# Kernel optimization log

Hardware: AMD Instinct MI355X
Metric: run time of the kernel (lower is better)

## Reference

```python
import jax, jax.numpy as jnp
import numpy as np

N_ENT = 40000
N_REL2 = 500      # num_rel * 2
E_DIR = 200000
E_2HOP = 50000
D_IN = 128        # entity/relation init dim
D_EMB = 256       # embed_dim
N_HEADS = 4
N_HID = D_EMB // N_HEADS  # 64
LRELU_ALPHA = 0.2
BN_EPS = 1e-5


def setup_inputs() -> dict:
    key = jax.random.key(0)
    ks = jax.random.split(key, 13)
    s = 0.1  # weight init scale
    return {
        "edge_index": jax.random.randint(ks[0], (2, E_DIR), 0, N_ENT),
        "edge_type": jax.random.randint(ks[1], (E_DIR,), 0, N_REL2),
        "indices_2hop": jax.random.randint(ks[2], (E_2HOP, 4), 0, N_REL2),
        "init_embed": jax.random.normal(ks[3], (N_ENT, D_IN), jnp.float32) * s,
        "init_rel": jax.random.normal(ks[4], (N_REL2, D_IN), jnp.float32) * s,
        "W_heads": jax.random.normal(ks[5], (N_HEADS, 2 * D_IN + D_IN, N_HID), jnp.float32) * s,
        "a_heads": jax.random.normal(ks[6], (N_HEADS, N_HID, 1), jnp.float32) * s,
        "gat_W": jax.random.normal(ks[7], (D_IN, D_EMB), jnp.float32) * s,
        "out_W": jax.random.normal(ks[8], (2 * D_EMB + D_EMB, D_EMB), jnp.float32) * s,
        "out_a": jax.random.normal(ks[9], (D_EMB, 1), jnp.float32) * s,
        "W_entities": jax.random.normal(ks[10], (D_IN, D_EMB), jnp.float32) * s,
        "bn_gamma": jnp.ones((D_EMB,), jnp.float32),
        "bn_beta": jnp.zeros((D_EMB,), jnp.float32),
    }


def segment_softmax(logits, idx, num_seg):
    # sparse softmax grouped by idx (PyG-style): subtract per-segment max, exp, normalize
    m = jax.ops.segment_max(logits, idx, num_segments=num_seg)
    e = jnp.exp(logits - m[idx])
    s = jax.ops.segment_sum(e, idx, num_segments=num_seg)
    return e / (s[idx] + 1e-16)


def reference(edge_index, edge_type, indices_2hop, init_embed, init_rel,
              W_heads, a_heads, gat_W, out_W, out_a, W_entities, bn_gamma, bn_beta):
    n = init_embed.shape[0]
    # build full edge list: flipped direct edges + 2-hop edges
    edge_nhop = jnp.stack([indices_2hop[:, 3], indices_2hop[:, 0]])  # [2, E2]
    ei = jnp.concatenate([edge_index[::-1], edge_nhop], axis=1)      # [2, Etot]
    row, col = ei[0], ei[1]
    t0, t1 = indices_2hop[:, 1], indices_2hop[:, 2]

    # first-layer edge relation embeddings
    edge_embed = jnp.concatenate([init_rel[edge_type], init_rel[t0] + init_rel[t1]], axis=0)
    feat = jnp.concatenate([init_embed[row], init_embed[col], edge_embed], axis=1)  # [Etot, 3*D_IN]

    def head(W, a):
        eh = feat @ W                                     # [Etot, N_HID]
        logit = jax.nn.leaky_relu((eh @ a)[:, 0], LRELU_ALPHA)
        alpha = segment_softmax(logit, row, n)
        agg = jax.ops.segment_sum(alpha[:, None] * eh, row, num_segments=n)
        return jax.nn.elu(agg)                            # concat=True -> elu

    x = jax.vmap(head)(W_heads, a_heads)                  # [H, N, N_HID]
    x = jnp.transpose(x, (1, 0, 2)).reshape(n, -1)        # [N, H*N_HID]

    r = init_rel @ gat_W                                  # [R2, D_EMB]
    edge_embed2 = jnp.concatenate([r[edge_type], r[t0] + r[t1]], axis=0)
    feat2 = jnp.concatenate([x[row], x[col], edge_embed2], axis=1)  # [Etot, 3*D_EMB]
    eh2 = feat2 @ out_W                                   # [Etot, D_EMB]
    logit2 = jax.nn.leaky_relu((eh2 @ out_a)[:, 0], LRELU_ALPHA)
    alpha2 = segment_softmax(logit2, row, n)
    out = jax.ops.segment_sum(alpha2[:, None] * eh2, row, num_segments=n)
    x = jax.nn.elu(out)                                   # elu applied in GAT.forward

    x = x + init_embed @ W_entities
    # BatchNorm1d (training-mode batch stats, biased variance)
    mu = jnp.mean(x, axis=0)
    var = jnp.var(x, axis=0)
    x = (x - mu) / jnp.sqrt(var + BN_EPS) * bn_gamma + bn_beta
    return x, r
```

## Files before the change

kernel.cpp:

```cpp
#include <hip/hip_runtime.h>
#include <hip/hip_bf16.h>
#include <math.h>

#define N_ENT 40000
#define N_REL 500
#define E_DIR 200000
#define E_2HOP 50000
#define E_TOT 250000
#define D_IN 128
#define D_EMB 256
#define LRELU 0.2f
#define BN_EPS 1e-5f
#define NB_SCAN 157
#define NB_DIR 782
#define NB2 8
#define E2PB 6250
#define N_HEAVY 500
#define DEG_SPLIT 32

typedef __hip_bfloat16 bf16;
typedef __attribute__((ext_vector_type(8))) short short8;
typedef __attribute__((ext_vector_type(4))) float float4v;

__device__ __forceinline__ float b2f(bf16 v){ return __bfloat162float(v); }
__device__ __forceinline__ float bitsf(unsigned int u){ return __builtin_bit_cast(float, u); }
__device__ __forceinline__ unsigned short bbits(float v){ return __builtin_bit_cast(unsigned short, __float2bfloat16(v)); }

__global__ void prep_hist(const float* __restrict__ Wh, const float* __restrict__ ow,
                          const float* __restrict__ we, const float* __restrict__ emb,
                          bf16* __restrict__ WAp, bf16* __restrict__ WBp, bf16* __restrict__ WEp,
                          bf16* __restrict__ OWp0, bf16* __restrict__ OWp1, float* __restrict__ WC,
                          bf16* __restrict__ embb,
                          const int* __restrict__ ei, const int* __restrict__ i2,
                          int* __restrict__ cnt, int* __restrict__ H2){
  __shared__ int hc[512];
  const int HS = 384*64;
  int b = blockIdx.x, tid = threadIdx.x;
  if (b < NB_DIR){
    int e = b*256 + tid;
    if (e < E_DIR) atomicAdd(&cnt[ei[E_DIR + e]], 1);
    return;
  }
  b -= NB_DIR;
  if (b < NB2){
    hc[tid] = 0; hc[tid + 256] = 0;
    __syncthreads();
    int base = b*E2PB;
    for (int it = 0; it < 25; it++){
      int o2 = it*256 + tid;
      if (o2 < E2PB){
        int r = i2[(base + o2)*4 + 3];
        atomicAdd(&hc[r], 1);
      }
    }
    __syncthreads();
    for (int r = tid; r < 500; r += 256) H2[b*500 + r] = hc[r];
    return;
  }
  b -= NB2;
  if (b >= 240){
    int i = (b - 240)*256 + tid;
    embb[i] = __float2bfloat16(emb[i]);
    return;
  }
  if (b < 112){
    int seg, base;
    if      (b < 16){ seg = 0; base = 0; }
    else if (b < 32){ seg = 1; base = 16; }
    else if (b < 48){ seg = 2; base = 32; }
    else if (b < 80){ seg = 3; base = 48; }
    else            { seg = 4; base = 80; }
    int idx = (b - base)*256 + tid;
    int lane = idx & 63, nt = (idx >> 6) & 15, kc = idx >> 10;
    int quad = lane >> 4, l16 = lane & 15;
    int col = nt*16 + l16;
    int kbase = kc*32 + quad*8;
    bf16* dst = (seg==0?WAp : seg==1?WBp : seg==2?WEp : seg==3?OWp0 : OWp1) + (size_t)idx*8;
    #pragma unroll
    for (int j = 0; j < 8; j++){
      int k = kbase + j;
      float v;
      if      (seg == 0) v = Wh[(col>>6)*HS + k*64 + (col&63)];
      else if (seg == 1) v = Wh[(col>>6)*HS + (k+128)*64 + (col&63)];
      else if (seg == 2) v = we[(size_t)k*256 + col];
      else if (seg == 3) v = ow[(size_t)k*256 + col];
      else               v = ow[(size_t)(k+256)*256 + col];
      dst[j] = __float2bfloat16(v);
    }
  } else {
    int idx = (b - 112)*256 + tid;
    int k = idx >> 8, col = idx & 255;
    WC[idx] = Wh[(col>>6)*HS + (k+256)*64 + (col&63)];
  }
}

__global__ void h2scan(const int* __restrict__ H2, int* __restrict__ b2off, int* __restrict__ c2){
  int r = threadIdx.x;
  if (r < 500){
    int s = 0;
    #pragma unroll
    for (int b = 0; b < NB2; b++){ b2off[b*500 + r] = s; s += H2[b*500 + r]; }
    c2[r] = s;
  }
}

__global__ void scan_bsum(const int* __restrict__ cnt, const int* __restrict__ c2,
                          int* __restrict__ bsum){
  int i = blockIdx.x*256 + threadIdx.x;
  int v = 0;
  if (i < N_ENT){ v = cnt[i]; if (i < 500) v += c2[i]; }
  int lane = threadIdx.x & 63, w = threadIdx.x >> 6;
  int s = v;
  #pragma unroll
  for (int o = 32; o >= 1; o >>= 1) s += __shfl_xor(s, o, 64);
  __shared__ int ws[4];
  if (lane == 0) ws[w] = s;
  __syncthreads();
  if (threadIdx.x == 0) bsum[blockIdx.x] = ws[0]+ws[1]+ws[2]+ws[3];
}

__global__ __launch_bounds__(256) void scan_final2(const int* __restrict__ cnt,
    const int* __restrict__ c2, const int* __restrict__ bsum, int* __restrict__ off){
  __shared__ int boffs[NB_SCAN];
  __shared__ int ws4[4];
  __shared__ int ws2[4];
  __shared__ int totals;
  int t = threadIdx.x;
  int lane = t & 63, w = t >> 6;
  {
    int v = (t < NB_SCAN) ? bsum[t] : 0;
    int s = v;
    #pragma unroll
    for (int o = 1; o < 64; o <<= 1){ int n = __shfl_up(s, o, 64); if (lane >= o) s += n; }
    if (lane == 63) ws4[w] = s;
    __syncthreads();
    int add = 0;
    for (int k = 0; k < w; k++) add += ws4[k];
    int incl = s + add;
    if (t < NB_SCAN) boffs[t] = incl - v;
    if (t == NB_SCAN-1) totals = incl;
  }
  __syncthreads();
  int i = blockIdx.x*256 + t;
  int v = 0;
  if (i < N_ENT){ v = cnt[i]; if (i < 500) v += c2[i]; }
  int s = v;
  #pragma unroll
  for (int o = 1; o < 64; o <<= 1){ int n = __shfl_up(s, o, 64); if (lane >= o) s += n; }
  if (lane == 63) ws2[w] = s;
  __syncthreads();
  int add = boffs[blockIdx.x];
  for (int k = 0; k < w; k++) add += ws2[k];
  if (i < N_ENT) off[i] = add + s - v;
  if (blockIdx.x == 0 && t == 0) off[N_ENT] = totals;
}

__device__ __forceinline__ void mfma_panel(const short* __restrict__ A,
    const short* __restrict__ Bp, bf16* __restrict__ C, int K,
    const float* __restrict__ avec, float* __restrict__ Sout, int dmode,
    int bx, int half){
  int w = threadIdx.x >> 6, lane = threadIdx.x & 63;
  int quad = lane >> 4, l16 = lane & 15;
  int rm = bx*64 + w*16;
  int arow = rm + l16;
  float4v acc[8];
  #pragma unroll
  for (int nt = 0; nt < 8; nt++) acc[nt] = (float4v){0.f,0.f,0.f,0.f};
  int nkc = K >> 5;
  const short8* Ap = (const short8*)(A + (size_t)arow*K);
  const short8* Bv = (const short8*)Bp + half*512 + lane;
  short8 a_cur = Ap[quad];
  for (int kc = 0; kc < nkc; kc++){
    int kn = (kc + 1 < nkc) ? kc + 1 : kc;
    short8 a_nxt = Ap[kn*4 + quad];
    const short8* bp = Bv + (size_t)kc*1024;
    short8 b[4];
    #pragma unroll
    for (int nt = 0; nt < 4; nt++) b[nt] = bp[nt*64];
    #pragma unroll
    for (int nt = 0; nt < 4; nt++)
      acc[nt] = __builtin_amdgcn_mfma_f32_16x16x32_bf16(a_cur, b[nt], acc[nt], 0, 0, 0);
    #pragma unroll
    for (int nt = 0; nt < 4; nt++) b[nt] = bp[(nt+4)*64];
    #pragma unroll
    for (int nt = 0; nt < 4; nt++)
      acc[nt+4] = __builtin_amdgcn_mfma_f32_16x16x32_bf16(a_cur, b[nt], acc[nt+4], 0, 0, 0);
    a_cur = a_nxt;
  }
  #pragma unroll
  for (int nt = 0; nt < 8; nt++){
    int col = (half*8 + nt)*16 + l16;
    #pragma unroll
    for (int r = 0; r < 4; r++)
      C[(size_t)(rm + quad*4 + r)*256 + col] = __float2bfloat16(acc[nt][r]);
  }
  if (Sout){
    if (dmode == 0){
      #pragma unroll
      for (int hl = 0; hl < 2; hl++){
        float pr[4] = {0.f,0.f,0.f,0.f};
        #pragma unroll
        for (int ntl = 0; ntl < 4; ntl++){
          int ln = hl*4 + ntl;
          float av = avec[(half*8 + ln)*16 + l16];
          #pragma unroll
          for (int r = 0; r < 4; r++) pr[r] += acc[ln][r]*av;
        }
        #pragma unroll
        for (int m = 8; m >= 1; m >>= 1)
          #pragma unroll
          for (int r = 0; r < 4; r++) pr[r] += __shfl_xor(pr[r], m, 64);
        if (l16 == 0){
          #pragma unroll
          for (int r = 0; r < 4; r++)
            Sout[(rm + quad*4 + r)*4 + half*2 + hl] = pr[r];
        }
      }
    } else {
      float pr[4] = {0.f,0.f,0.f,0.f};
      #pragma unroll
      for (int ln = 0; ln < 8; ln++){
        float av = avec[(half*8 + ln)*16 + l16];
        #pragma unroll
        for (int r = 0; r < 4; r++) pr[r] += acc[ln][r]*av;
      }
      #pragma unroll
      for (int m = 8; m >= 1; m >>= 1)
        #pragma unroll
        for (int r = 0; r < 4; r++) pr[r] += __shfl_xor(pr[r], m, 64);
      if (l16 == 0){
        #pragma unroll
        for (int r = 0; r < 4; r++) atomicAdd(&Sout[rm + quad*4 + r], pr[r]);
      }
    }
  }
}

__device__ __forceinline__ void gemm64_body(const float* __restrict__ A,
    const float* __restrict__ B, float* __restrict__ C, bf16* __restrict__ Cb,
    int M, int K, const float* __restrict__ av, float* __restrict__ So, int mode,
    int bxx, int byy, char* smem){
  const int N = 256;
  float (*As)[65] = (float (*)[65])smem;
  float (*Bsf)[65] = (float (*)[65])(smem + 16*65*sizeof(float));
  int bm = bxx * 64, bn = byy * 64;
  int tid = threadIdx.x;
  int tx = tid & 15, ty = tid >> 4;
  float acc[4][4] = {};
  for (int k0 = 0; k0 < K; k0 += 16){
    #pragma unroll
    for (int j = 0; j < 4; j++){
      int idx = tid + j*256;
      int m = idx >> 4, kk = idx & 15;
      int gm = bm + m;
      float v = 0.f;
      if (gm < M) v = A[(size_t)gm*K + k0 + kk];
      As[kk][m] = v;
    }
    #pragma unroll
    for (int j = 0; j < 4; j++){
      int idx = tid + j*256;
      int kk = idx >> 6, n = idx & 63;
      Bsf[kk][n] = B[(size_t)(k0+kk)*N + bn + n];
    }
    __syncthreads();
    #pragma unroll
    for (int kk = 0; kk < 16; kk++){
      float a[4], b[4];
      #pragma unroll
      for (int i = 0; i < 4; i++) a[i] = As[kk][ty*4+i];
      #pragma unroll
      for (int j = 0; j < 4; j++) b[j] = Bsf[kk][tx*4+j];
      #pragma unroll
      for (int i = 0; i < 4; i++)
        #pragma unroll
        for (int j = 0; j < 4; j++) acc[i][j] += a[i]*b[j];
    }
    __syncthreads();
  }
  if (Cb){
    #pragma unroll
    for (int i = 0; i < 4; i++){
      int gm = bm + ty*4 + i;
      if (gm >= M) continue;
      #pragma unroll
      for (int j = 0; j < 4; j++)
        Cb[(size_t)gm*N + bn + tx*4 + j] = __float2bfloat16(acc[i][j]);
    }
  } else {
    #pragma unroll
    for (int i = 0; i < 4; i++){
      int gm = bm + ty*4 + i;
      if (gm >= M) continue;
      #pragma unroll
      for (int j = 0; j < 4; j++)
        C[(size_t)gm*N + bn + tx*4 + j] = acc[i][j];
    }
  }
  if (mode != 2){
    float pr[4];
    #pragma unroll
    for (int i = 0; i < 4; i++){
      float p = 0.f;
      #pragma unroll
      for (int j = 0; j < 4; j++) p += acc[i][j]*av[bn + tx*4 + j];
      pr[i] = p;
    }
    #pragma unroll
    for (int m = 8; m >= 1; m >>= 1)
      #pragma unroll
      for (int i = 0; i < 4; i++) pr[i] += __shfl_xor(pr[i], m, 64);
    if (tx == 0){
      #pragma unroll
      for (int i = 0; i < 4; i++){
        int gm = bm + ty*4 + i;
        if (gm < M){
          if (mode == 0) So[gm*4 + byy] = pr[i];
          else atomicAdd(&So[gm], pr[i]);
        }
      }
    }
  }
}

__global__ __launch_bounds__(256, 4) void mega1(
    const short* __restrict__ embb, const short* __restrict__ WAp, const short* __restrict__ WBp,
    const short* __restrict__ WEp, bf16* __restrict__ P1, bf16* __restrict__ P2, bf16* __restrict__ EP,
    const float* __restrict__ ah, float* __restrict__ S1, float* __restrict__ S2,
    const float* __restrict__ rel, const float* __restrict__ WC, const float* __restrict__ gw,
    float* __restrict__ RF, float* __restrict__ SRm, bf16* __restrict__ PRb,
    const int* __restrict__ ei, const int* __restrict__ et, const int* __restrict__ i2,
    const int* __restrict__ off, int* __restrict__ cur, const int* __restrict__ b2off,
    int4* __restrict__ EIDX, int useEP){
  __shared__ char smem[8704];
  __shared__ int lc[512];
  int x = blockIdx.x, tid = threadIdx.x;
  if (x < NB_DIR){
    int e = x*256 + tid;
    if (e < E_DIR){
      int r = ei[E_DIR + e];
      int p = atomicAdd(&cur[r], 1);
      int4 v; v.x = ei[e]; v.y = et[e]; v.z = -1; v.w = r;
      EIDX[off[r] + p] = v;
    }
    return;
  }
  x -= NB_DIR;
  if (x < NB2){
    lc[tid] = 0; lc[tid + 256] = 0;
    __syncthreads();
    int base = x*E2PB;
    for (int it = 0; it < 25; it++){
      int o2 = it*256 + tid;
      if (o2 < E2PB){
        int e2 = base + o2;
        int q = e2*4;
        int r = i2[q + 3];
        int myp = atomicAdd(&lc[r], 1);
        int d = off[r+1] - 1 - (b2off[x*500 + r] + myp);
        int4 v; v.x = i2[q]; v.y = i2[q+1]; v.z = i2[q+2]; v.w = r;
        EIDX[d] = v;
      }
    }
    return;
  }
  x -= NB2;
  if (x < 64){
    int z = x >> 5, rr = x & 31, by = rr >> 3, bx = rr & 7;
    if (z == 0) gemm64_body(rel, WC, nullptr, PRb, N_REL, 128, ah, SRm, 0, bx, by, smem);
    else        gemm64_body(rel, gw, RF, nullptr, N_REL, 128, nullptr, nullptr, 2, bx, by, smem);
    return;
  }
  x -= 64;
  int p = x / 1250, rest = x % 1250;
  if (p == 2 && !useEP) return;
  const short* B = p==0 ? WAp : (p==1 ? WBp : WEp);
  bf16* C = p==0 ? P1 : (p==1 ? P2 : EP);
  float* S = p==0 ? S1 : (p==1 ? S2 : nullptr);
  mfma_panel(embb, B, C, 128, ah, S, 0, rest >> 1, rest & 1);
}

__global__ __launch_bounds__(256, 4) void mega2(
    const short* __restrict__ X1s, const short* __restrict__ OWp0, const short* __restrict__ OWp1,
    bf16* __restrict__ Q1, bf16* __restrict__ Q2, const float* __restrict__ oa,
    float* __restrict__ S1B, float* __restrict__ S2B,
    const float* __restrict__ RF, const float* __restrict__ owB, float* __restrict__ SRB,
    bf16* __restrict__ QRb){
  __shared__ char smem[8704];
  int x = blockIdx.x;
  if (x < 32){
    int by = x >> 3, bx = x & 7;
    gemm64_body(RF, owB, nullptr, QRb, N_REL, 256, oa, SRB, 1, bx, by, smem);
    return;
  }
  x -= 32;
  int p = x / 1250, rest = x % 1250;
  mfma_panel(X1s, p==0 ? OWp0 : OWp1, p==0 ? Q1 : Q2, 256, oa,
             p==0 ? S1B : S2B, 1, rest >> 1, rest & 1);
}

__global__ void gemm64_acc(const float* __restrict__ A, const float* __restrict__ B,
                           float* __restrict__ C, int M, int K){
  const int N = 256;
  __shared__ float As[16][65];
  __shared__ float Bs[16][65];
  int bm = blockIdx.x * 64, bn = blockIdx.y * 64;
  int tid = threadIdx.x;
  int tx = tid & 15, ty = tid >> 4;
  float acc[4][4] = {};
  for (int k0 = 0; k0 < K; k0 += 16){
    #pragma unroll
    for (int j = 0; j < 4; j++){
      int idx = tid + j*256;
      int m = idx >> 4, kk = idx & 15;
      int gm = bm + m;
      float v = 0.f;
      if (gm < M) v = A[(size_t)gm*K + k0 + kk];
      As[kk][m] = v;
    }
    #pragma unroll
    for (int j = 0; j < 4; j++){
      int idx = tid + j*256;
      int kk = idx >> 6, n = idx & 63;
      Bs[kk][n] = B[(size_t)(k0+kk)*N + bn + n];
    }
    __syncthreads();
    #pragma unroll
    for (int kk = 0; kk < 16; kk++){
      float a[4], b[4];
      #pragma unroll
      for (int i = 0; i < 4; i++) a[i] = As[kk][ty*4+i];
      #pragma unroll
      for (int j = 0; j < 4; j++) b[j] = Bs[kk][tx*4+j];
      #pragma unroll
      for (int i = 0; i < 4; i++)
        #pragma unroll
        for (int j = 0; j < 4; j++) acc[i][j] += a[i]*b[j];
    }
    __syncthreads();
  }
  #pragma unroll
  for (int i = 0; i < 4; i++){
    int gm = bm + ty*4 + i;
    if (gm >= M) continue;
    #pragma unroll
    for (int j = 0; j < 4; j++){
      size_t o = (size_t)gm*N + bn + tx*4 + j;
      C[o] += acc[i][j];
    }
  }
}

__global__ __launch_bounds__(256) void sm1f(const int* __restrict__ off, const int4* __restrict__ EIDX,
    const float* __restrict__ s1, const float* __restrict__ s2, const float* __restrict__ sR,
    float* __restrict__ L1, float* __restrict__ AS1, float* __restrict__ IV1){
  if (blockIdx.x < N_HEAVY){
    int i = blockIdx.x;
    int st = off[i], en = off[i+1];
    if (en - st <= DEG_SPLIT) return;
    int h = threadIdx.x >> 6, lane = threadIdx.x & 63;
    float* Lh = L1 + (size_t)h*E_TOT;
    float si = s1[i*4 + h];
    float mx = -1e30f;
    for (int t = st + lane; t < en; t += 64){
      int4 e = EIDX[t];
      float v = si + s2[e.x*4+h] + sR[e.y*4+h];
      if (e.z >= 0) v += sR[e.z*4+h];
      v = (v >= 0.f) ? v : LRELU*v;
      Lh[t] = v;
      mx = fmaxf(mx, v);
    }
    #pragma unroll
    for (int o = 32; o >= 1; o >>= 1) mx = fmaxf(mx, __shfl_xor(mx, o, 64));
    float sm = 0.f;
    for (int t = st + lane; t < en; t += 64){
      float ev = __expf(Lh[t] - mx); Lh[t] = ev; sm += ev;
    }
    #pragma unroll
    for (int o = 32; o >= 1; o >>= 1) sm += __shfl_xor(sm, o, 64);
    float inv = 1.f/(sm + 1e-16f);
    if (lane == 0){ AS1[i*4+h] = sm*inv; IV1[i*4+h] = inv; }
    return;
  }
  int wid = threadIdx.x >> 6, lane = threadIdx.x & 63;
  int i = (blockIdx.x - N_HEAVY)*4 + wid;
  if (i >= N_ENT) return;
  int st = off[i], en = off[i+1];
  if (i < N_HEAVY && en - st > DEG_SPLIT) return;
  int hf = lane >> 4, l16 = lane & 15;
  float* Lh = L1 + (size_t)hf*E_TOT;
  float si = s1[i*4 + hf];
  if (en - st > 2*16){
    float mx = -1e30f;
    for (int t = st + l16; t < en; t += 16){
      int4 e = EIDX[t];
      float v = si + s2[e.x*4+hf] + sR[e.y*4+hf];
      if (e.z >= 0) v += sR[e.z*4+hf];
      v = (v >= 0.f) ? v : LRELU*v;
      Lh[t] = v; mx = fmaxf(mx, v);
    }
    #pragma unroll
    for (int o = 8; o >= 1; o >>= 1) mx = fmaxf(mx, __shfl_xor(mx, o, 64));
    float sm = 0.f;
    for (int t = st + l16; t < en; t += 16){
      float ev = __expf(Lh[t] - mx); Lh[t] = ev; sm += ev;
    }
    #pragma unroll
    for (int o = 8; o >= 1; o >>= 1) sm += __shfl_xor(sm, o, 64);
    float inv = 1.f/(sm + 1e-16f);
    if (l16 == 0){ AS1[i*4+hf] = sm*inv; IV1[i*4+hf] = inv; }
    return;
  }
  int t0 = st + l16, t1 = t0 + 16;
  float v0 = -1e30f, v1 = -1e30f;
  if (t0 < en){
    int4 e = EIDX[t0];
    float v = si + s2[e.x*4+hf] + sR[e.y*4+hf];
    if (e.z >= 0) v += sR[e.z*4+hf];
    v0 = (v >= 0.f) ? v : LRELU*v;
  }
  if (t1 < en){
    int4 e = EIDX[t1];
    float v = si + s2[e.x*4+hf] + sR[e.y*4+hf];
    if (e.z >= 0) v += sR[e.z*4+hf];
    v1 = (v >= 0.f) ? v : LRELU*v;
  }
  float mx = fmaxf(v0, v1);
  #pragma unroll
  for (int o = 8; o >= 1; o >>= 1) mx = fmaxf(mx, __shfl_xor(mx, o, 64));
  float sm = 0.f;
  if (t0 < en){ float ev = __expf(v0 - mx); Lh[t0] = ev; sm += ev; }
  if (t1 < en){ float ev = __expf(v1 - mx); Lh[t1] = ev; sm += ev; }
  #pragma unroll
  for (int o = 8; o >= 1; o >>= 1) sm += __shfl_xor(sm, o, 64);
  float inv = 1.f/(sm + 1e-16f);
  if (l16 == 0){ AS1[i*4+hf] = sm*inv; IV1[i*4+hf] = inv; }
}

__global__ __launch_bounds__(256) void sm2f(const int* __restrict__ off, const int4* __restrict__ EIDX,
    const float* __restrict__ s1, const float* __restrict__ s2, const float* __restrict__ sR,
    float* __restrict__ L2, float* __restrict__ AS2, float* __restrict__ IV2){
  __shared__ float wsm[4], wss[4];
  if (blockIdx.x < N_HEAVY){
    int i = blockIdx.x;
    int st = off[i], en = off[i+1];
    if (en - st <= DEG_SPLIT) return;
    int tid = threadIdx.x, w = tid >> 6, lane = tid & 63;
    float si = s1[i];
    float mx = -1e30f;
    for (int t = st + tid; t < en; t += 256){
      int4 e = EIDX[t];
      float v = si + s2[e.x] + sR[e.y];
      if (e.z >= 0) v += sR[e.z];
      v = (v >= 0.f) ? v : LRELU*v;
      L2[t] = v; mx = fmaxf(mx, v);
    }
    #pragma unroll
    for (int o = 32; o >= 1; o >>= 1) mx = fmaxf(mx, __shfl_xor(mx, o, 64));
    if (lane == 0) wsm[w] = mx;
    __syncthreads();
    mx = fmaxf(fmaxf(wsm[0], wsm[1]), fmaxf(wsm[2], wsm[3]));
    float sm = 0.f;
    for (int t = st + tid; t < en; t += 256){
      float ev = __expf(L2[t] - mx); L2[t] = ev; sm += ev;
    }
    #pragma unroll
    for (int o = 32; o >= 1; o >>= 1) sm += __shfl_xor(sm, o, 64);
    if (lane == 0) wss[w] = sm;
    __syncthreads();
    sm = wss[0]+wss[1]+wss[2]+wss[3];
    float inv = 1.f/(sm + 1e-16f);
    if (tid == 0){ AS2[i] = sm*inv; IV2[i] = inv; }
    return;
  }
  int wid = threadIdx.x >> 6, lane = threadIdx.x & 63;
  int i = (blockIdx.x - N_HEAVY)*4 + wid;
  if (i >= N_ENT) return;
  int st = off[i], en = off[i+1];
  if (i < N_HEAVY && en - st > DEG_SPLIT) return;
  float si = s1[i];
  if (en - st > 64){
    float mx = -1e30f;
    for (int t = st + lane; t < en; t += 64){
      int4 e = EIDX[t];
      float v = si + s2[e.x] + sR[e.y];
      if (e.z >= 0) v += sR[e.z];
      v = (v >= 0.f) ? v : LRELU*v;
      L2[t] = v; mx = fmaxf(mx, v);
    }
    #pragma unroll
    for (int o = 32; o >= 1; o >>= 1) mx = fmaxf(mx, __shfl_xor(mx, o, 64));
    float sm = 0.f;
    for (int t = st + lane; t < en; t += 64){
      float ev = __expf(L2[t] - mx); L2[t] = ev; sm += ev;
    }
    #pragma unroll
    for (int o = 32; o >= 1; o >>= 1) sm += __shfl_xor(sm, o, 64);
    float inv = 1.f/(sm + 1e-16f);
    if (lane == 0){ AS2[i] = sm*inv; IV2[i] = inv; }
    return;
  }
  int t0 = st + lane;
  float v0 = -1e30f;
  if (t0 < en){
    int4 e = EIDX[t0];
    float v = si + s2[e.x] + sR[e.y];
    if (e.z >= 0) v += sR[e.z];
    v0 = (v >= 0.f) ? v : LRELU*v;
  }
  float mx = v0;
  #pragma unroll
  for (int o = 32; o >= 1; o >>= 1) mx = fmaxf(mx, __shfl_xor(mx, o, 64));
  float sm = 0.f;
  if (t0 < en){ float ev = __expf(v0 - mx); L2[t0] = ev; sm += ev; }
  #pragma unroll
  for (int o = 32; o >= 1; o >>= 1) sm += __shfl_xor(sm, o, 64);
  float inv = 1.f/(sm + 1e-16f);
  if (lane == 0){ AS2[i] = sm*inv; IV2[i] = inv; }
}

#define UNPK(u, r0, r1, r2, r3) \
  r0 = bitsf((u).x << 16); r1 = bitsf((u).x & 0xffff0000u); \
  r2 = bitsf((u).y << 16); r3 = bitsf((u).y & 0xffff0000u);

__global__ __launch_bounds__(256) void agg1(const int* __restrict__ off,
    const int4* __restrict__ EIDX, const float* __restrict__ W1, const float* __restrict__ AS1,
    const float* __restrict__ IV1,
    const bf16* __restrict__ P1, const bf16* __restrict__ P2, const bf16* __restrict__ PRm,
    bf16* __restrict__ X1){
  __shared__ float red[4][256];
  if (blockIdx.x < N_HEAVY){
    int i = blockIdx.x;
    int st = off[i], en = off[i+1];
    if (en - st <= DEG_SPLIT) return;
    int w = threadIdx.x >> 6, lane = threadIdx.x & 63;
    int hf = lane >> 4, f0 = lane*4;
    size_t ob = (size_t)i*256 + f0;
    const float* Wp = W1 + (size_t)hf*E_TOT;
    float a0=0,a1=0,a2=0,a3=0;
    for (int t = st + w*4; t < en; t += 16){
      int4 e[4]; float wv[4]; uint2 u[4]; uint2 rr[4];
      #pragma unroll
      for (int k = 0; k < 4; k++){
        int tt = t + k;
        bool vld = tt < en;
        int tc = vld ? tt : st;
        e[k] = EIDX[tc]; wv[k] = vld ? Wp[tc] : 0.f;
      }
      #pragma unroll
      for (int k = 0; k < 4; k++){
        u[k] = *(const uint2*)(P2 + (size_t)e[k].x*256 + f0);
        rr[k] = *(const uint2*)(PRm + (size_t)e[k].y*256 + f0);
      }
      float rf[4][4];
      #pragma unroll
      for (int k = 0; k < 4; k++){ UNPK(rr[k], rf[k][0], rf[k][1], rf[k][2], rf[k][3]) }
      #pragma unroll
      for (int k = 0; k < 4; k++){
        if (e[k].z >= 0){
          uint2 s = *(const uint2*)(PRm + (size_t)e[k].z*256 + f0);
          float s0,s1,s2,s3; UNPK(s, s0,s1,s2,s3)
          rf[k][0] += s0; rf[k][1] += s1; rf[k][2] += s2; rf[k][3] += s3;
        }
      }
      #pragma unroll
      for (int k = 0; k < 4; k++){
        a0 += wv[k]*(bitsf(u[k].x << 16) + rf[k][0]);
        a1 += wv[k]*(bitsf(u[k].x & 0xffff0000u) + rf[k][1]);
        a2 += wv[k]*(bitsf(u[k].y << 16) + rf[k][2]);
        a3 += wv[k]*(bitsf(u[k].y & 0xffff0000u) + rf[k][3]);
      }
    }
    *(float4*)&red[w][f0] = (float4){a0, a1, a2, a3};
    __syncthreads();
    if (w == 0){
      float4 r1 = *(float4*)&red[1][f0];
      float4 r2 = *(float4*)&red[2][f0];
      float4 r3 = *(float4*)&red[3][f0];
      a0 += r1.x + r2.x + r3.x;
      a1 += r1.y + r2.y + r3.y;
      a2 += r1.z + r2.z + r3.z;
      a3 += r1.w + r2.w + r3.w;
      float iv = IV1[i*4 + hf];
      a0 *= iv; a1 *= iv; a2 *= iv; a3 *= iv;
      float as = AS1[i*4 + hf];
      uint2 up = *(const uint2*)(P1 + ob);
      a0 += as*bitsf(up.x << 16);
      a1 += as*bitsf(up.x & 0xffff0000u);
      a2 += as*bitsf(up.y << 16);
      a3 += as*bitsf(up.y & 0xffff0000u);
      a0 = (a0 > 0.f) ? a0 : __expf(a0)-1.f;
      a1 = (a1 > 0.f) ? a1 : __expf(a1)-1.f;
      a2 = (a2 > 0.f) ? a2 : __expf(a2)-1.f;
      a3 = (a3 > 0.f) ? a3 : __expf(a3)-1.f;
      unsigned int lo = (unsigned int)bbits(a0) | ((unsigned int)bbits(a1) << 16);
      unsigned int hi = (unsigned int)bbits(a2) | ((unsigned int)bbits(a3) << 16);
      *(uint2*)(X1 + ob) = (uint2){lo, hi};
    }
    return;
  }
  int wid = threadIdx.x >> 6, lane = threadIdx.x & 63;
  int i = (blockIdx.x - N_HEAVY)*4 + wid;
  if (i >= N_ENT) return;
  int st = off[i], en = off[i+1];
  if (i < N_HEAVY && en - st > DEG_SPLIT) return;
  int hf = lane >> 4, f0 = lane*4;
  size_t ob = (size_t)i*256 + f0;
  if (st == en){
    *(uint2*)(X1 + ob) = (uint2){0u, 0u};
    return;
  }
  const float* Wp = W1 + (size_t)hf*E_TOT;
  float a0=0,a1=0,a2=0,a3=0;
  int t = st;
  int n4 = st + ((en - st) & ~3);
  for (; t < n4; t += 4){
    int4 e[4]; float wv[4]; uint2 u[4]; uint2 rr[4];
    #pragma unroll
    for (int k = 0; k < 4; k++){ e[k] = EIDX[t+k]; wv[k] = Wp[t+k]; }
    #pragma unroll
    for (int k = 0; k < 4; k++){
      u[k] = *(const uint2*)(P2 + (size_t)e[k].x*256 + f0);
      rr[k] = *(const uint2*)(PRm + (size_t)e[k].y*256 + f0);
    }
    float rf[4][4];
    #pragma unroll
    for (int k = 0; k < 4; k++){ UNPK(rr[k], rf[k][0], rf[k][1], rf[k][2], rf[k][3]) }
    #pragma unroll
    for (int k = 0; k < 4; k++){
      if (e[k].z >= 0){
        uint2 s = *(const uint2*)(PRm + (size_t)e[k].z*256 + f0);
        float s0,s1,s2,s3; UNPK(s, s0,s1,s2,s3)
        rf[k][0] += s0; rf[k][1] += s1; rf[k][2] += s2; rf[k][3] += s3;
      }
    }
    #pragma unroll
    for (int k = 0; k < 4; k++){
      a0 += wv[k]*(bitsf(u[k].x << 16) + rf[k][0]);
      a1 += wv[k]*(bitsf(u[k].x & 0xffff0000u) + rf[k][1]);
      a2 += wv[k]*(bitsf(u[k].y << 16) + rf[k][2]);
      a3 += wv[k]*(bitsf(u[k].y & 0xffff0000u) + rf[k][3]);
    }
  }
  for (; t < en; t++){
    float w = Wp[t];
    int4 e = EIDX[t];
    uint2 u = *(const uint2*)(P2 + (size_t)e.x*256 + f0);
    uint2 rr = *(const uint2*)(PRm + (size_t)e.y*256 + f0);
    float r0,r1,r2,r3; UNPK(rr, r0,r1,r2,r3)
    if (e.z >= 0){
      uint2 s = *(const uint2*)(PRm + (size_t)e.z*256 + f0);
      float s0,s1,s2,s3; UNPK(s, s0,s1,s2,s3)
      r0 += s0; r1 += s1; r2 += s2; r3 += s3;
    }
    a0 += w*(bitsf(u.x << 16) + r0);
    a1 += w*(bitsf(u.x & 0xffff0000u) + r1);
    a2 += w*(bitsf(u.y << 16) + r2);
    a3 += w*(bitsf(u.y & 0xffff0000u) + r3);
  }
  float iv = IV1[i*4 + hf];
  a0 *= iv; a1 *= iv; a2 *= iv; a3 *= iv;
  float as = AS1[i*4 + hf];
  uint2 up = *(const uint2*)(P1 + ob);
  a0 += as*bitsf(up.x << 16);
  a1 += as*bitsf(up.x & 0xffff0000u);
  a2 += as*bitsf(up.y << 16);
  a3 += as*bitsf(up.y & 0xffff0000u);
  a0 = (a0 > 0.f) ? a0 : __expf(a0)-1.f;
  a1 = (a1 > 0.f) ? a1 : __expf(a1)-1.f;
  a2 = (a2 > 0.f) ? a2 : __expf(a2)-1.f;
  a3 = (a3 > 0.f) ? a3 : __expf(a3)-1.f;
  unsigned int lo = (unsigned int)bbits(a0) | ((unsigned int)bbits(a1) << 16);
  unsigned int hi = (unsigned int)bbits(a2) | ((unsigned int)bbits(a3) << 16);
  *(uint2*)(X1 + ob) = (uint2){lo, hi};
}

__global__ __launch_bounds__(256) void agg2(const int* __restrict__ off,
    const int4* __restrict__ EIDX, const float* __restrict__ W2, const float* __restrict__ AS2,
    const float* __restrict__ IV2,
    const bf16* __restrict__ Q1, const bf16* __restrict__ Q2, const bf16* __restrict__ QRm,
    const bf16* __restrict__ EP, float* __restrict__ X2){
  __shared__ float red[4][256];
  if (blockIdx.x < N_HEAVY){
    int i = blockIdx.x;
    int st = off[i], en = off[i+1];
    if (en - st <= DEG_SPLIT) return;
    int w = threadIdx.x >> 6, lane = threadIdx.x & 63;
    int f0 = lane*4;
    size_t ob = (size_t)i*256 + f0;
    float a0=0,a1=0,a2=0,a3=0;
    for (int t = st + w*4; t < en; t += 16){
      int4 e[4]; float wv[4]; uint2 u[4]; uint2 rr[4];
      #pragma unroll
      for (int k = 0; k < 4; k++){
        int tt = t + k;
        bool vld = tt < en;
        int tc = vld ? tt : st;
        e[k] = EIDX[tc]; wv[k] = vld ? W2[tc] : 0.f;
      }
      #pragma unroll
      for (int k = 0; k < 4; k++){
        u[k] = *(const uint2*)(Q2 + (size_t)e[k].x*256 + f0);
        rr[k] = *(const uint2*)(QRm + (size_t)e[k].y*256 + f0);
      }
      float rf[4][4];
      #pragma unroll
      for (int k = 0; k < 4; k++){ UNPK(rr[k], rf[k][0], rf[k][1], rf[k][2], rf[k][3]) }
      #pragma unroll
      for (int k = 0; k < 4; k++){
        if (e[k].z >= 0){
          uint2 s = *(const uint2*)(QRm + (size_t)e[k].z*256 + f0);
          float s0,s1,s2,s3; UNPK(s, s0,s1,s2,s3)
          rf[k][0] += s0; rf[k][1] += s1; rf[k][2] += s2; rf[k][3] += s3;
        }
      }
      #pragma unroll
      for (int k = 0; k < 4; k++){
        a0 += wv[k]*(bitsf(u[k].x << 16) + rf[k][0]);
        a1 += wv[k]*(bitsf(u[k].x & 0xffff0000u) + rf[k][1]);
        a2 += wv[k]*(bitsf(u[k].y << 16) + rf[k][2]);
        a3 += wv[k]*(bitsf(u[k].y & 0xffff0000u) + rf[k][3]);
      }
    }
    *(float4*)&red[w][f0] = (float4){a0, a1, a2, a3};
    __syncthreads();
    if (w == 0){
      float4 r1 = *(float4*)&red[1][f0];
      float4 r2 = *(float4*)&red[2][f0];
      float4 r3 = *(float4*)&red[3][f0];
      a0 += r1.x + r2.x + r3.x;
      a1 += r1.y + r2.y + r3.y;
      a2 += r1.z + r2.z + r3.z;
      a3 += r1.w + r2.w + r3.w;
      float iv = IV2[i];
      a0 *= iv; a1 *= iv; a2 *= iv; a3 *= iv;
      float ep0=0.f, ep1=0.f, ep2=0.f, ep3=0.f;
      if (EP){
        uint2 ue = *(const uint2*)(EP + ob);
        ep0 = bitsf(ue.x << 16); ep1 = bitsf(ue.x & 0xffff0000u);
        ep2 = bitsf(ue.y << 16); ep3 = bitsf(ue.y & 0xffff0000u);
      }
      float as = AS2[i];
      uint2 uq = *(const uint2*)(Q1 + ob);
      a0 += as*bitsf(uq.x << 16);
      a1 += as*bitsf(uq.x & 0xffff0000u);
      a2 += as*bitsf(uq.y << 16);
      a3 += as*bitsf(uq.y & 0xffff0000u);
      a0 = ((a0 > 0.f) ? a0 : __expf(a0)-1.f) + ep0;
      a1 = ((a1 > 0.f) ? a1 : __expf(a1)-1.f) + ep1;
      a2 = ((a2 > 0.f) ? a2 : __expf(a2)-1.f) + ep2;
      a3 = ((a3 > 0.f) ? a3 : __expf(a3)-1.f) + ep3;
      *(float4*)(X2 + ob) = (float4){a0, a1, a2, a3};
    }
    return;
  }
  int wid = threadIdx.x >> 6, lane = threadIdx.x & 63;
  int i = (blockIdx.x - N_HEAVY)*4 + wid;
  if (i >= N_ENT) return;
  int st = off[i], en = off[i+1];
  if (i < N_HEAVY && en - st > DEG_SPLIT) return;
  int f0 = lane*4;
  size_t ob = (size_t)i*256 + f0;
  float ep0=0.f, ep1=0.f, ep2=0.f, ep3=0.f;
  if (EP){
    uint2 ue = *(const uint2*)(EP + ob);
    ep0 = bitsf(ue.x << 16); ep1 = bitsf(ue.x & 0xffff0000u);
    ep2 = bitsf(ue.y << 16); ep3 = bitsf(ue.y & 0xffff0000u);
  }
  if (st == en){
    *(float4*)(X2 + ob) = (float4){ep0, ep1, ep2, ep3};
    return;
  }
  float a0=0,a1=0,a2=0,a3=0;
  int t = st;
  int n4 = st + ((en - st) & ~3);
  for (; t < n4; t += 4){
    int4 e[4]; float wv[4]; uint2 u[4]; uint2 rr[4];
    #pragma unroll
    for (int k = 0; k < 4; k++){ e[k] = EIDX[t+k]; wv[k] = W2[t+k]; }
    #pragma unroll
    for (int k = 0; k < 4; k++){
      u[k] = *(const uint2*)(Q2 + (size_t)e[k].x*256 + f0);
      rr[k] = *(const uint2*)(QRm + (size_t)e[k].y*256 + f0);
    }
    float rf[4][4];
    #pragma unroll
    for (int k = 0; k < 4; k++){ UNPK(rr[k], rf[k][0], rf[k][1], rf[k][2], rf[k][3]) }
    #pragma unroll
    for (int k = 0; k < 4; k++){
      if (e[k].z >= 0){
        uint2 s = *(const uint2*)(QRm + (size_t)e[k].z*256 + f0);
        float s0,s1,s2,s3; UNPK(s, s0,s1,s2,s3)
        rf[k][0] += s0; rf[k][1] += s1; rf[k][2] += s2; rf[k][3] += s3;
      }
    }
    #pragma unroll
    for (int k = 0; k < 4; k++){
      a0 += wv[k]*(bitsf(u[k].x << 16) + rf[k][0]);
      a1 += wv[k]*(bitsf(u[k].x & 0xffff0000u) + rf[k][1]);
      a2 += wv[k]*(bitsf(u[k].y << 16) + rf[k][2]);
      a3 += wv[k]*(bitsf(u[k].y & 0xffff0000u) + rf[k][3]);
    }
  }
  for (; t < en; t++){
    float w = W2[t];
    int4 e = EIDX[t];
    uint2 u = *(const uint2*)(Q2 + (size_t)e.x*256 + f0);
    uint2 rr = *(const uint2*)(QRm + (size_t)e.y*256 + f0);
    float r0,r1,r2,r3; UNPK(rr, r0,r1,r2,r3)
    if (e.z >= 0){
      uint2 s = *(const uint2*)(QRm + (size_t)e.z*256 + f0);
      float s0,s1,s2,s3; UNPK(s, s0,s1,s2,s3)
      r0 += s0; r1 += s1; r2 += s2; r3 += s3;
    }
    a0 += w*(bitsf(u.x << 16) + r0);
    a1 += w*(bitsf(u.x & 0xffff0000u) + r1);
    a2 += w*(bitsf(u.y << 16) + r2);
    a3 += w*(bitsf(u.y & 0xffff0000u) + r3);
  }
  float iv = IV2[i];
  a0 *= iv; a1 *= iv; a2 *= iv; a3 *= iv;
  float as = AS2[i];
  uint2 uq = *(const uint2*)(Q1 + ob);
  a0 += as*bitsf(uq.x << 16);
  a1 += as*bitsf(uq.x & 0xffff0000u);
  a2 += as*bitsf(uq.y << 16);
  a3 += as*bitsf(uq.y & 0xffff0000u);
  a0 = ((a0 > 0.f) ? a0 : __expf(a0)-1.f) + ep0;
  a1 = ((a1 > 0.f) ? a1 : __expf(a1)-1.f) + ep1;
  a2 = ((a2 > 0.f) ? a2 : __expf(a2)-1.f) + ep2;
  a3 = ((a3 > 0.f) ? a3 : __expf(a3)-1.f) + ep3;
  *(float4*)(X2 + ob) = (float4){a0, a1, a2, a3};
}

__global__ void bn_reduce(const float* __restrict__ X, float* __restrict__ sums, float* __restrict__ sq){
  int ch = threadIdx.x;
  float s = 0.f, q = 0.f;
  for (int r = blockIdx.x; r < N_ENT; r += gridDim.x){
    float v = X[(size_t)r*256 + ch];
    s += v; q += v*v;
  }
  atomicAdd(&sums[ch], s);
  atomicAdd(&sq[ch], q);
}

__global__ void bn_final_r(float* __restrict__ X, const float* __restrict__ sums, const float* __restrict__ sq,
                           const float* __restrict__ gamma, const float* __restrict__ beta,
                           const float* __restrict__ RF, float* __restrict__ out_r){
  int b = blockIdx.x;
  if (b < 40000){
    int idx = b*256 + threadIdx.x;
    int ch = idx & 255;
    const float invn = 1.f/(float)N_ENT;
    float mean = sums[ch] * invn;
    float var  = fmaxf(sq[ch] * invn - mean*mean, 0.f);
    X[idx] = (X[idx] - mean) * rsqrtf(var + BN_EPS) * gamma[ch] + beta[ch];
  } else {
    int idx = (b - 40000)*256 + threadIdx.x;
    out_r[idx] = RF[idx];
  }
}

extern "C" void kernel_launch(void* const* d_in, const int* in_sizes, int n_in,
                              void* d_out, int out_size, void* d_ws, size_t ws_size,
                              hipStream_t stream){
  const int*   ei  = (const int*)d_in[0];
  const int*   et  = (const int*)d_in[1];
  const int*   i2  = (const int*)d_in[2];
  const float* emb = (const float*)d_in[3];
  const float* rel = (const float*)d_in[4];
  const float* Wh  = (const float*)d_in[5];
  const float* ah  = (const float*)d_in[6];
  const float* gw  = (const float*)d_in[7];
  const float* ow  = (const float*)d_in[8];
  const float* oa  = (const float*)d_in[9];
  const float* we  = (const float*)d_in[10];
  const float* gma = (const float*)d_in[11];
  const float* bta = (const float*)d_in[12];
  float* out = (float*)d_out;

  char* ws = (char*)d_ws;
  size_t o = 0;
  auto alloc = [&](size_t bytes)->char*{
    char* p = ws + o; o = (o + bytes + 255) & ~(size_t)255; return p;
  };
  bf16*  P1  = (bf16*)alloc(20480000);
  bf16*  P2  = (bf16*)alloc(20480000);
  bf16*  PRb = (bf16*)alloc(256000);
  bf16*  QRb = (bf16*)alloc(256000);
  float* RF  = (float*)alloc(512000);
  float* WC  = (float*)alloc(131072);
  bf16*  WAp = (bf16*)alloc(65536);
  bf16*  WBp = (bf16*)alloc(65536);
  bf16*  WEp = (bf16*)alloc(65536);
  bf16*  OWp0= (bf16*)alloc(131072);
  bf16*  OWp1= (bf16*)alloc(131072);
  float* S1  = (float*)alloc(640000);
  float* S2  = (float*)alloc(640000);
  float* SRm = (float*)alloc(8192);
  float* S1B = (float*)alloc(160000);
  float* S2B = (float*)alloc(160000);
  int*   CNT = (int*)alloc(160000);
  int*   CUR = (int*)alloc(160000);
  float* SRB = (float*)alloc(2048);
  float* BNS = (float*)alloc(1024);
  float* BNQ = (float*)alloc(1024);
  int*   OFF = (int*)alloc(160016);
  int*   BSUM= (int*)alloc(1024);
  int*   H2  = (int*)alloc(16000);
  int*   B2O = (int*)alloc(16000);
  int*   C2  = (int*)alloc(2048);
  int4*  EIDX= (int4*)alloc(4000000);
  float* L1  = (float*)alloc(4000000);
  float* L2  = (float*)alloc(1000000);
  float* AS1 = (float*)alloc(640000);
  float* AS2 = (float*)alloc(160000);
  float* IV1 = (float*)alloc(640000);
  float* IV2 = (float*)alloc(160000);
  size_t base_end = o;
  bool useEP = (ws_size >= base_end + 20480256 + 512);
  bf16* EP = nullptr;
  if (useEP) EP = (bf16*)alloc(20480000);
  bf16* X1b  = (bf16*)out;
  bf16* embb = (bf16*)((char*)out + 20480000);
  float* X2 = out;
  (void)in_sizes; (void)n_in; (void)out_size;

  hipMemsetAsync(S1B, 0, 644096, stream);

  prep_hist<<<NB_DIR + NB2 + 20240, 256, 0, stream>>>(Wh, ow, we, emb,
      WAp, WBp, WEp, OWp0, OWp1, WC, embb, ei, i2, CNT, H2);

  h2scan<<<1, 512, 0, stream>>>(H2, B2O, C2);
  scan_bsum<<<NB_SCAN, 256, 0, stream>>>(CNT, C2, BSUM);
  scan_final2<<<NB_SCAN, 256, 0, stream>>>(CNT, C2, BSUM, OFF);

  mega1<<<NB_DIR + NB2 + 64 + 3750, 256, 0, stream>>>(
      (const short*)embb, (const short*)WAp, (const short*)WBp, (const short*)WEp,
      P1, P2, EP, ah, S1, S2,
      rel, WC, gw, RF, SRm, PRb,
      ei, et, i2, OFF, CUR, B2O, EIDX, useEP ? 1 : 0);

  sm1f<<<N_HEAVY + N_ENT/4, 256, 0, stream>>>(OFF, EIDX, S1, S2, SRm, L1, AS1, IV1);
  agg1<<<N_HEAVY + N_ENT/4, 256, 0, stream>>>(OFF, EIDX, L1, AS1, IV1, P1, P2, PRb, X1b);

  mega2<<<32 + 2500, 256, 0, stream>>>(
      (const short*)X1b, (const short*)OWp0, (const short*)OWp1,
      P1, P2, oa, S1B, S2B, RF, ow + 131072, SRB, QRb);

  sm2f<<<N_HEAVY + N_ENT/4, 256, 0, stream>>>(OFF, EIDX, S1B, S2B, SRB, L2, AS2, IV2);
  agg2<<<N_HEAVY + N_ENT/4, 256, 0, stream>>>(OFF, EIDX, L2, AS2, IV2, P1, P2, QRb, EP, X2);

  if (!useEP)
    gemm64_acc<<<dim3((N_ENT+63)/64, 4), 256, 0, stream>>>(emb, we, X2, N_ENT, 128);

  bn_reduce<<<1024, 256, 0, stream>>>(X2, BNS, BNQ);
  bn_final_r<<<40500, 256, 0, stream>>>(X2, BNS, BNQ, gma, bta, RF, out + (size_t)N_ENT*256);
}
```

Before: 373.9 us.

## Fuse segment softmax into aggregation kernels for both GAT layers

Result: faster. 353.2 us (-5.5%).

```diff
diff --git a/kernel.cpp b/kernel.cpp
--- a/kernel.cpp
+++ b/kernel.cpp
@@ -17,6 +17,8 @@
 #define E2PB 6250
 #define N_HEAVY 500
 #define DEG_SPLIT 32
+#define HM1 512
+#define HM2 1024
 
 typedef __hip_bfloat16 bf16;
 typedef __attribute__((ext_vector_type(8))) short short8;
@@ -451,35 +453,131 @@
   }
 }
 
-__global__ __launch_bounds__(256) void sm1f(const int* __restrict__ off, const int4* __restrict__ EIDX,
+#define UNPK(u, r0, r1, r2, r3) \
+  r0 = bitsf((u).x << 16); r1 = bitsf((u).x & 0xffff0000u); \
+  r2 = bitsf((u).y << 16); r3 = bitsf((u).y & 0xffff0000u);
+
+__global__ __launch_bounds__(256) void fag1(const int* __restrict__ off,
+    const int4* __restrict__ EIDX,
     const float* __restrict__ s1, const float* __restrict__ s2, const float* __restrict__ sR,
-    float* __restrict__ L1, float* __restrict__ AS1, float* __restrict__ IV1){
+    const bf16* __restrict__ P1, const bf16* __restrict__ P2, const bf16* __restrict__ PRm,
+    bf16* __restrict__ X1){
+  __shared__ float red[4][256];
+  __shared__ float wE[4][HM1];
+  __shared__ float hsum[4], hmx[4];
   if (blockIdx.x < N_HEAVY){
     int i = blockIdx.x;
     int st = off[i], en = off[i+1];
     if (en - st <= DEG_SPLIT) return;
-    int h = threadIdx.x >> 6, lane = threadIdx.x & 63;
-    float* Lh = L1 + (size_t)h*E_TOT;
-    float si = s1[i*4 + h];
-    float mx = -1e30f;
-    for (int t = st + lane; t < en; t += 64){
-      int4 e = EIDX[t];
-      float v = si + s2[e.x*4+h] + sR[e.y*4+h];
-      if (e.z >= 0) v += sR[e.z*4+h];
-      v = (v >= 0.f) ? v : LRELU*v;
-      Lh[t] = v;
-      mx = fmaxf(mx, v);
-    }
-    #pragma unroll
-    for (int o = 32; o >= 1; o >>= 1) mx = fmaxf(mx, __shfl_xor(mx, o, 64));
-    float sm = 0.f;
-    for (int t = st + lane; t < en; t += 64){
-      float ev = __expf(Lh[t] - mx); Lh[t] = ev; sm += ev;
-    }
-    #pragma unroll
-    for (int o = 32; o >= 1; o >>= 1) sm += __shfl_xor(sm, o, 64);
-    float inv = 1.f/(sm + 1e-16f);
-    if (lane == 0){ AS1[i*4+h] = sm*inv; IV1[i*4+h] = inv; }
+    int w = threadIdx.x >> 6, lane = threadIdx.x & 63;
+    {
+      float si = s1[i*4 + w];
+      float mx = -1e30f;
+      for (int t = st + lane; t < en; t += 64){
+        int4 e = EIDX[t];
+        float v = si + s2[e.x*4+w] + sR[e.y*4+w];
+        if (e.z >= 0) v += sR[e.z*4+w];
+        v = (v >= 0.f) ? v : LRELU*v;
+        int idx = t - st;
+        if (idx < HM1) wE[w][idx] = v;
+        mx = fmaxf(mx, v);
+      }
+      #pragma unroll
+      for (int o = 32; o >= 1; o >>= 1) mx = fmaxf(mx, __shfl_xor(mx, o, 64));
+      float sm = 0.f;
+      for (int t = st + lane; t < en; t += 64){
+        int idx = t - st;
+        float v;
+        if (idx < HM1) v = wE[w][idx];
+        else {
+          int4 e = EIDX[t];
+          v = si + s2[e.x*4+w] + sR[e.y*4+w];
+          if (e.z >= 0) v += sR[e.z*4+w];
+          v = (v >= 0.f) ? v : LRELU*v;
+        }
+        float ev = __expf(v - mx);
+        if (idx < HM1) wE[w][idx] = ev;
+        sm += ev;
+      }
+      #pragma unroll
+      for (int o = 32; o >= 1; o >>= 1) sm += __shfl_xor(sm, o, 64);
+      if (lane == 0){ hsum[w] = sm; hmx[w] = mx; }
+    }
+    __syncthreads();
+    int hf = lane >> 4, f0 = lane*4;
+    size_t ob = (size_t)i*256 + f0;
+    float si2 = s1[i*4 + hf], mxh = hmx[hf];
+    float a0=0,a1=0,a2=0,a3=0;
+    for (int t = st + w*4; t < en; t += 16){
+      int4 e[4]; float wv[4]; uint2 u[4]; uint2 rr[4];
+      #pragma unroll
+      for (int k = 0; k < 4; k++){
+        int tt = t + k;
+        bool vld = tt < en;
+        int tc = vld ? tt : st;
+        e[k] = EIDX[tc];
+        int idx = tc - st;
+        float wt;
+        if (idx < HM1) wt = wE[hf][idx];
+        else {
+          float v = si2 + s2[e[k].x*4+hf] + sR[e[k].y*4+hf];
+          if (e[k].z >= 0) v += sR[e[k].z*4+hf];
+          v = (v >= 0.f) ? v : LRELU*v;
+          wt = __expf(v - mxh);
+        }
+        wv[k] = vld ? wt : 0.f;
+      }
+      #pragma unroll
+      for (int k = 0; k < 4; k++){
+        u[k] = *(const uint2*)(P2 + (size_t)e[k].x*256 + f0);
+        rr[k] = *(const uint2*)(PRm + (size_t)e[k].y*256 + f0);
+      }
+      float rf[4][4];
+      #pragma unroll
+      for (int k = 0; k < 4; k++){ UNPK(rr[k], rf[k][0], rf[k][1], rf[k][2], rf[k][3]) }
+      #pragma unroll
+      for (int k = 0; k < 4; k++){
+        if (e[k].z >= 0){
+          uint2 s = *(const uint2*)(PRm + (size_t)e[k].z*256 + f0);
+          float s0,ss1,ss2,s3; UNPK(s, s0,ss1,ss2,s3)
+          rf[k][0] += s0; rf[k][1] += ss1; rf[k][2] += ss2; rf[k][3] += s3;
+        }
+      }
+      #pragma unroll
+      for (int k = 0; k < 4; k++){
+        a0 += wv[k]*(bitsf(u[k].x << 16) + rf[k][0]);
+        a1 += wv[k]*(bitsf(u[k].x & 0xffff0000u) + rf[k][1]);
+        a2 += wv[k]*(bitsf(u[k].y << 16) + rf[k][2]);
+        a3 += wv[k]*(bitsf(u[k].y & 0xffff0000u) + rf[k][3]);
+      }
+    }
+    *(float4*)&red[w][f0] = (float4){a0, a1, a2, a3};
+    __syncthreads();
+    if (w == 0){
+      float4 r1 = *(float4*)&red[1][f0];
+      float4 r2 = *(float4*)&red[2][f0];
+      float4 r3 = *(float4*)&red[3][f0];
+      a0 += r1.x + r2.x + r3.x;
+      a1 += r1.y + r2.y + r3.y;
+      a2 += r1.z + r2.z + r3.z;
+      a3 += r1.w + r2.w + r3.w;
+      float sm = hsum[hf];
+      float iv = 1.f/(sm + 1e-16f);
+      float as = sm*iv;
+      a0 *= iv; a1 *= iv; a2 *= iv; a3 *= iv;
+      uint2 up = *(const uint2*)(P1 + ob);
+      a0 += as*bitsf(up.x << 16);
+      a1 += as*bitsf(up.x & 0xffff0000u);
+      a2 += as*bitsf(up.y << 16);
+      a3 += as*bitsf(up.y & 0xffff0000u);
+      a0 = (a0 > 0.f) ? a0 : __expf(a0)-1.f;
+      a1 = (a1 > 0.f) ? a1 : __expf(a1)-1.f;
+      a2 = (a2 > 0.f) ? a2 : __expf(a2)-1.f;
+      a3 = (a3 > 0.f) ? a3 : __expf(a3)-1.f;
+      unsigned int lo = (unsigned int)bbits(a0) | ((unsigned int)bbits(a1) << 16);
+      unsigned int hi = (unsigned int)bbits(a2) | ((unsigned int)bbits(a3) << 16);
+      *(uint2*)(X1 + ob) = (uint2){lo, hi};
+    }
     return;
   }
   int wid = threadIdx.x >> 6, lane = threadIdx.x & 63;
@@ -487,59 +585,160 @@
   if (i >= N_ENT) return;
   int st = off[i], en = off[i+1];
   if (i < N_HEAVY && en - st > DEG_SPLIT) return;
-  int hf = lane >> 4, l16 = lane & 15;
-  float* Lh = L1 + (size_t)hf*E_TOT;
+  int hf = lane >> 4, l16 = lane & 15, f0 = lane*4;
+  size_t ob = (size_t)i*256 + f0;
+  if (st == en){
+    *(uint2*)(X1 + ob) = (uint2){0u, 0u};
+    return;
+  }
   float si = s1[i*4 + hf];
-  if (en - st > 2*16){
+  int deg = en - st;
+  float a0=0,a1=0,a2=0,a3=0;
+  float iv, as;
+  if (deg <= 32){
+    int t0 = st + l16, t1 = t0 + 16;
+    float v0 = -1e30f, v1 = -1e30f;
+    if (t0 < en){
+      int4 e = EIDX[t0];
+      float v = si + s2[e.x*4+hf] + sR[e.y*4+hf];
+      if (e.z >= 0) v += sR[e.z*4+hf];
+      v0 = (v >= 0.f) ? v : LRELU*v;
+    }
+    if (t1 < en){
+      int4 e = EIDX[t1];
+      float v = si + s2[e.x*4+hf] + sR[e.y*4+hf];
+      if (e.z >= 0) v += sR[e.z*4+hf];
+      v1 = (v >= 0.f) ? v : LRELU*v;
+    }
+    float mx = fmaxf(v0, v1);
+    #pragma unroll
+    for (int o = 8; o >= 1; o >>= 1) mx = fmaxf(mx, __shfl_xor(mx, o, 64));
+    float ev0 = (t0 < en) ? __expf(v0 - mx) : 0.f;
+    float ev1 = (t1 < en) ? __expf(v1 - mx) : 0.f;
+    float sm = ev0 + ev1;
+    #pragma unroll
+    for (int o = 8; o >= 1; o >>= 1) sm += __shfl_xor(sm, o, 64);
+    iv = 1.f/(sm + 1e-16f);
+    as = sm*iv;
+    int t = st;
+    int n4 = st + (deg & ~3);
+    for (; t < n4; t += 4){
+      int j = t - st;
+      int4 e[4]; float wv[4]; uint2 u[4]; uint2 rr[4];
+      #pragma unroll
+      for (int k = 0; k < 4; k++){
+        e[k] = EIDX[t+k];
+        int jj = j + k;
+        wv[k] = (jj < 16) ? __shfl(ev0, hf*16 + jj, 64)
+                          : __shfl(ev1, hf*16 + jj - 16, 64);
+      }
+      #pragma unroll
+      for (int k = 0; k < 4; k++){
+        u[k] = *(const uint2*)(P2 + (size_t)e[k].x*256 + f0);
+        rr[k] = *(const uint2*)(PRm + (size_t)e[k].y*256 + f0);
+      }
+      float rf[4][4];
+      #pragma unroll
+      for (int k = 0; k < 4; k++){ UNPK(rr[k], rf[k][0], rf[k][1], rf[k][2], rf[k][3]) }
+      #pragma unroll
+      for (int k = 0; k < 4; k++){
+        if (e[k].z >= 0){
+          uint2 s = *(const uint2*)(PRm + (size_t)e[k].z*256 + f0);
+          float s0,ss1,ss2,s3; UNPK(s, s0,ss1,ss2,s3)
+          rf[k][0] += s0; rf[k][1] += ss1; rf[k][2] += ss2; rf[k][3] += s3;
+        }
+      }
+      #pragma unroll
+      for (int k = 0; k < 4; k++){
+        a0 += wv[k]*(bitsf(u[k].x << 16) + rf[k][0]);
+        a1 += wv[k]*(bitsf(u[k].x & 0xffff0000u) + rf[k][1]);
+        a2 += wv[k]*(bitsf(u[k].y << 16) + rf[k][2]);
+        a3 += wv[k]*(bitsf(u[k].y & 0xffff0000u) + rf[k][3]);
+      }
+    }
+    for (; t < en; t++){
+      int j = t - st;
+      float w = (j < 16) ? __shfl(ev0, hf*16 + j, 64)
+                         : __shfl(ev1, hf*16 + j - 16, 64);
+      int4 e = EIDX[t];
+      uint2 u = *(const uint2*)(P2 + (size_t)e.x*256 + f0);
+      uint2 rr = *(const uint2*)(PRm + (size_t)e.y*256 + f0);
+      float r0,r1,r2,r3; UNPK(rr, r0,r1,r2,r3)
+      if (e.z >= 0){
+        uint2 s = *(const uint2*)(PRm + (size_t)e.z*256 + f0);
+        float s0,ss1,ss2,s3; UNPK(s, s0,ss1,ss2,s3)
+        r0 += s0; r1 += ss1; r2 += ss2; r3 += s3;
+      }
+      a0 += w*(bitsf(u.x << 16) + r0);
+      a1 += w*(bitsf(u.x & 0xffff0000u) + r1);
+      a2 += w*(bitsf(u.y << 16) + r2);
+      a3 += w*(bitsf(u.y & 0xffff0000u) + r3);
+    }
+  } else {
     float mx = -1e30f;
     for (int t = st + l16; t < en; t += 16){
       int4 e = EIDX[t];
       float v = si + s2[e.x*4+hf] + sR[e.y*4+hf];
       if (e.z >= 0) v += sR[e.z*4+hf];
       v = (v >= 0.f) ? v : LRELU*v;
-      Lh[t] = v; mx = fmaxf(mx, v);
+      mx = fmaxf(mx, v);
     }
     #pragma unroll
     for (int o = 8; o >= 1; o >>= 1) mx = fmaxf(mx, __shfl_xor(mx, o, 64));
     float sm = 0.f;
     for (int t = st + l16; t < en; t += 16){
-      float ev = __expf(Lh[t] - mx); Lh[t] = ev; sm += ev;
+      int4 e = EIDX[t];
+      float v = si + s2[e.x*4+hf] + sR[e.y*4+hf];
+      if (e.z >= 0) v += sR[e.z*4+hf];
+      v = (v >= 0.f) ? v : LRELU*v;
+      sm += __expf(v - mx);
     }
     #pragma unroll
     for (int o = 8; o >= 1; o >>= 1) sm += __shfl_xor(sm, o, 64);
-    float inv = 1.f/(sm + 1e-16f);
-    if (l16 == 0){ AS1[i*4+hf] = sm*inv; IV1[i*4+hf] = inv; }
-    return;
-  }
-  int t0 = st + l16, t1 = t0 + 16;
-  float v0 = -1e30f, v1 = -1e30f;
-  if (t0 < en){
-    int4 e = EIDX[t0];
-    float v = si + s2[e.x*4+hf] + sR[e.y*4+hf];
-    if (e.z >= 0) v += sR[e.z*4+hf];
-    v0 = (v >= 0.f) ? v : LRELU*v;
-  }
-  if (t1 < en){
-    int4 e = EIDX[t1];
-    float v = si + s2[e.x*4+hf] + sR[e.y*4+hf];
-    if (e.z >= 0) v += sR[e.z*4+hf];
-    v1 = (v >= 0.f) ? v : LRELU*v;
-  }
-  float mx = fmaxf(v0, v1);
-  #pragma unroll
-  for (int o = 8; o >= 1; o >>= 1) mx = fmaxf(mx, __shfl_xor(mx, o, 64));
-  float sm = 0.f;
-  if (t0 < en){ float ev = __expf(v0 - mx); Lh[t0] = ev; sm += ev; }
-  if (t1 < en){ float ev = __expf(v1 - mx); Lh[t1] = ev; sm += ev; }
-  #pragma unroll
-  for (int o = 8; o >= 1; o >>= 1) sm += __shfl_xor(sm, o, 64);
-  float inv = 1.f/(sm + 1e-16f);
-  if (l16 == 0){ AS1[i*4+hf] = sm*inv; IV1[i*4+hf] = inv; }
-}
-
-__global__ __launch_bounds__(256) void sm2f(const int* __restrict__ off, const int4* __restrict__ EIDX,
+    iv = 1.f/(sm + 1e-16f);
+    as = sm*iv;
+    for (int t = st; t < en; t++){
+      int4 e = EIDX[t];
+      float v = si + s2[e.x*4+hf] + sR[e.y*4+hf];
+      if (e.z >= 0) v += sR[e.z*4+hf];
+      v = (v >= 0.f) ? v : LRELU*v;
+      float w = __expf(v - mx);
+      uint2 u = *(const uint2*)(P2 + (size_t)e.x*256 + f0);
+      uint2 rr = *(const uint2*)(PRm + (size_t)e.y*256 + f0);
+      float r0,r1,r2,r3; UNPK(rr, r0,r1,r2,r3)
+      if (e.z >= 0){
+        uint2 s = *(const uint2*)(PRm + (size_t)e.z*256 + f0);
+        float s0,ss1,ss2,s3; UNPK(s, s0,ss1,ss2,s3)
+        r0 += s0; r1 += ss1; r2 += ss2; r3 += s3;
+      }
+      a0 += w*(bitsf(u.x << 16) + r0);
+      a1 += w*(bitsf(u.x & 0xffff0000u) + r1);
+      a2 += w*(bitsf(u.y << 16) + r2);
+      a3 += w*(bitsf(u.y & 0xffff0000u) + r3);
+    }
+  }
+  a0 *= iv; a1 *= iv; a2 *= iv; a3 *= iv;
+  uint2 up = *(const uint2*)(P1 + ob);
+  a0 += as*bitsf(up.x << 16);
+  a1 += as*bitsf(up.x & 0xffff0000u);
+  a2 += as*bitsf(up.y << 16);
+  a3 += as*bitsf(up.y & 0xffff0000u);
+  a0 = (a0 > 0.f) ? a0 : __expf(a0)-1.f;
+  a1 = (a1 > 0.f) ? a1 : __expf(a1)-1.f;
+  a2 = (a2 > 0.f) ? a2 : __expf(a2)-1.f;
+  a3 = (a3 > 0.f) ? a3 : __expf(a3)-1.f;
+  unsigned int lo = (unsigned int)bbits(a0) | ((unsigned int)bbits(a1) << 16);
+  unsigned int hi = (unsigned int)bbits(a2) | ((unsigned int)bbits(a3) << 16);
+  *(uint2*)(X1 + ob) = (uint2){lo, hi};
+}
+
+__global__ __launch_bounds__(256) void fag2(const int* __restrict__ off,
+    const int4* __restrict__ EIDX,
     const float* __restrict__ s1, const float* __restrict__ s2, const float* __restrict__ sR,
-    float* __restrict__ L2, float* __restrict__ AS2, float* __restrict__ IV2){
+    const bf16* __restrict__ Q1, const bf16* __restrict__ Q2, const bf16* __restrict__ QRm,
+    const bf16* __restrict__ EP, float* __restrict__ X2){
+  __shared__ float red[4][256];
+  __shared__ float wE2[HM2];
   __shared__ float wsm[4], wss[4];
   if (blockIdx.x < N_HEAVY){
     int i = blockIdx.x;
@@ -553,7 +752,9 @@
       float v = si + s2[e.x] + sR[e.y];
       if (e.z >= 0) v += sR[e.z];
       v = (v >= 0.f) ? v : LRELU*v;
-      L2[t] = v; mx = fmaxf(mx, v);
+      int idx = t - st;
+      if (idx < HM2) wE2[idx] = v;
+      mx = fmaxf(mx, v);
     }
     #pragma unroll
     for (int o = 32; o >= 1; o >>= 1) mx = fmaxf(mx, __shfl_xor(mx, o, 64));
@@ -562,81 +763,28 @@
     mx = fmaxf(fmaxf(wsm[0], wsm[1]), fmaxf(wsm[2], wsm[3]));
     float sm = 0.f;
     for (int t = st + tid; t < en; t += 256){
-      float ev = __expf(L2[t] - mx); L2[t] = ev; sm += ev;
+      int idx = t - st;
+      float v;
+      if (idx < HM2) v = wE2[idx];
+      else {
+        int4 e = EIDX[t];
+        v = si + s2[e.x] + sR[e.y];
+        if (e.z >= 0) v += sR[e.z];
+        v = (v >= 0.f) ? v : LRELU*v;
+      }
+      float ev = __expf(v - mx);
+      if (idx < HM2) wE2[idx] = ev;
+      sm += ev;
     }
     #pragma unroll
     for (int o = 32; o >= 1; o >>= 1) sm += __shfl_xor(sm, o, 64);
     if (lane == 0) wss[w] = sm;
     __syncthreads();
     sm = wss[0]+wss[1]+wss[2]+wss[3];
-    float inv = 1.f/(sm + 1e-16f);
-    if (tid == 0){ AS2[i] = sm*inv; IV2[i] = inv; }
-    return;
-  }
-  int wid = threadIdx.x >> 6, lane = threadIdx.x & 63;
-  int i = (blockIdx.x - N_HEAVY)*4 + wid;
-  if (i >= N_ENT) return;
-  int st = off[i], en = off[i+1];
-  if (i < N_HEAVY && en - st > DEG_SPLIT) return;
-  float si = s1[i];
-  if (en - st > 64){
-    float mx = -1e30f;
-    for (int t = st + lane; t < en; t += 64){
-      int4 e = EIDX[t];
-      float v = si + s2[e.x] + sR[e.y];
-      if (e.z >= 0) v += sR[e.z];
-      v = (v >= 0.f) ? v : LRELU*v;
-      L2[t] = v; mx = fmaxf(mx, v);
-    }
-    #pragma unroll
-    for (int o = 32; o >= 1; o >>= 1) mx = fmaxf(mx, __shfl_xor(mx, o, 64));
-    float sm = 0.f;
-    for (int t = st + lane; t < en; t += 64){
-      float ev = __expf(L2[t] - mx); L2[t] = ev; sm += ev;
-    }
-    #pragma unroll
-    for (int o = 32; o >= 1; o >>= 1) sm += __shfl_xor(sm, o, 64);
-    float inv = 1.f/(sm + 1e-16f);
-    if (lane == 0){ AS2[i] = sm*inv; IV2[i] = inv; }
-    return;
-  }
-  int t0 = st + lane;
-  float v0 = -1e30f;
-  if (t0 < en){
-    int4 e = EIDX[t0];
-    float v = si + s2[e.x] + sR[e.y];
-    if (e.z >= 0) v += sR[e.z];
-    v0 = (v >= 0.f) ? v : LRELU*v;
-  }
-  float mx = v0;
-  #pragma unroll
-  for (int o = 32; o >= 1; o >>= 1) mx = fmaxf(mx, __shfl_xor(mx, o, 64));
-  float sm = 0.f;
-  if (t0 < en){ float ev = __expf(v0 - mx); L2[t0] = ev; sm += ev; }
-  #pragma unroll
-  for (int o = 32; o >= 1; o >>= 1) sm += __shfl_xor(sm, o, 64);
-  float inv = 1.f/(sm + 1e-16f);
-  if (lane == 0){ AS2[i] = sm*inv; IV2[i] = inv; }
-}
-
-#define UNPK(u, r0, r1, r2, r3) \
-  r0 = bitsf((u).x << 16); r1 = bitsf((u).x & 0xffff0000u); \
-  r2 = bitsf((u).y << 16); r3 = bitsf((u).y & 0xffff0000u);
-
-__global__ __launch_bounds__(256) void agg1(const int* __restrict__ off,
-    const int4* __restrict__ EIDX, const float* __restrict__ W1, const float* __restrict__ AS1,
-    const float* __restrict__ IV1,
-    const bf16* __restrict__ P1, const bf16* __restrict__ P2, const bf16* __restrict__ PRm,
-    bf16* __restrict__ X1){
-  __shared__ float red[4][256];
-  if (blockIdx.x < N_HEAVY){
-    int i = blockIdx.x;
-    int st = off[i], en = off[i+1];
-    if (en - st <= DEG_SPLIT) return;
-    int w = threadIdx.x >> 6, lane = threadIdx.x & 63;
-    int hf = lane >> 4, f0 = lane*4;
+    float iv = 1.f/(sm + 1e-16f);
+    float as = sm*iv;
+    int f0 = lane*4;
     size_t ob = (size_t)i*256 + f0;
-    const float* Wp = W1 + (size_t)hf*E_TOT;
     float a0=0,a1=0,a2=0,a3=0;
     for (int t = st + w*4; t < en; t += 16){
       int4 e[4]; float wv[4]; uint2 u[4]; uint2 rr[4];
@@ -645,12 +793,22 @@
         int tt = t + k;
         bool vld = tt < en;
         int tc = vld ? tt : st;
-        e[k] = EIDX[tc]; wv[k] = vld ? Wp[tc] : 0.f;
-      }
-      #pragma unroll
-      for (int k = 0; k < 4; k++){
-        u[k] = *(const uint2*)(P2 + (size_t)e[k].x*256 + f0);
-        rr[k] = *(const uint2*)(PRm + (size_t)e[k].y*256 + f0);
+        e[k] = EIDX[tc];
+        int idx = tc - st;
+        float wt;
+        if (idx < HM2) wt = wE2[idx];
+        else {
+          float v = si + s2[e[k].x] + sR[e[k].y];
+          if (e[k].z >= 0) v += sR[e[k].z];
+          v = (v >= 0.f) ? v : LRELU*v;
+          wt = __expf(v - mx);
+        }
+        wv[k] = vld ? wt : 0.f;
+      }
+      #pragma unroll
+      for (int k = 0; k < 4; k++){
+        u[k] = *(const uint2*)(Q2 + (size_t)e[k].x*256 + f0);
+        rr[k] = *(const uint2*)(QRm + (size_t)e[k].y*256 + f0);
       }
       float rf[4][4];
       #pragma unroll
@@ -658,9 +816,9 @@
       #pragma unroll
       for (int k = 0; k < 4; k++){
         if (e[k].z >= 0){
-          uint2 s = *(const uint2*)(PRm + (size_t)e[k].z*256 + f0);
-          float s0,s1,s2,s3; UNPK(s, s0,s1,s2,s3)
-          rf[k][0] += s0; rf[k][1] += s1; rf[k][2] += s2; rf[k][3] += s3;
+          uint2 s = *(const uint2*)(QRm + (size_t)e[k].z*256 + f0);
+          float s0,ss1,ss2,s3; UNPK(s, s0,ss1,ss2,s3)
+          rf[k][0] += s0; rf[k][1] += ss1; rf[k][2] += ss2; rf[k][3] += s3;
         }
       }
       #pragma unroll
@@ -681,158 +839,6 @@
       a1 += r1.y + r2.y + r3.y;
       a2 += r1.z + r2.z + r3.z;
       a3 += r1.w + r2.w + r3.w;
-      float iv = IV1[i*4 + hf];
-      a0 *= iv; a1 *= iv; a2 *= iv; a3 *= iv;
-      float as = AS1[i*4 + hf];
-      uint2 up = *(const uint2*)(P1 + ob);
-      a0 += as*bitsf(up.x << 16);
-      a1 += as*bitsf(up.x & 0xffff0000u);
-      a2 += as*bitsf(up.y << 16);
-      a3 += as*bitsf(up.y & 0xffff0000u);
-      a0 = (a0 > 0.f) ? a0 : __expf(a0)-1.f;
-      a1 = (a1 > 0.f) ? a1 : __expf(a1)-1.f;
-      a2 = (a2 > 0.f) ? a2 : __expf(a2)-1.f;
-      a3 = (a3 > 0.f) ? a3 : __expf(a3)-1.f;
-      unsigned int lo = (unsigned int)bbits(a0) | ((unsigned int)bbits(a1) << 16);
-      unsigned int hi = (unsigned int)bbits(a2) | ((unsigned int)bbits(a3) << 16);
-      *(uint2*)(X1 + ob) = (uint2){lo, hi};
-    }
-    return;
-  }
-  int wid = threadIdx.x >> 6, lane = threadIdx.x & 63;
-  int i = (blockIdx.x - N_HEAVY)*4 + wid;
-  if (i >= N_ENT) return;
-  int st = off[i], en = off[i+1];
-  if (i < N_HEAVY && en - st > DEG_SPLIT) return;
-  int hf = lane >> 4, f0 = lane*4;
-  size_t ob = (size_t)i*256 + f0;
-  if (st == en){
-    *(uint2*)(X1 + ob) = (uint2){0u, 0u};
-    return;
-  }
-  const float* Wp = W1 + (size_t)hf*E_TOT;
-  float a0=0,a1=0,a2=0,a3=0;
-  int t = st;
-  int n4 = st + ((en - st) & ~3);
-  for (; t < n4; t += 4){
-    int4 e[4]; float wv[4]; uint2 u[4]; uint2 rr[4];
-    #pragma unroll
-    for (int k = 0; k < 4; k++){ e[k] = EIDX[t+k]; wv[k] = Wp[t+k]; }
-    #pragma unroll
-    for (int k = 0; k < 4; k++){
-      u[k] = *(const uint2*)(P2 + (size_t)e[k].x*256 + f0);
-      rr[k] = *(const uint2*)(PRm + (size_t)e[k].y*256 + f0);
-    }
-    float rf[4][4];
-    #pragma unroll
-    for (int k = 0; k < 4; k++){ UNPK(rr[k], rf[k][0], rf[k][1], rf[k][2], rf[k][3]) }
-    #pragma unroll
-    for (int k = 0; k < 4; k++){
-      if (e[k].z >= 0){
-        uint2 s = *(const uint2*)(PRm + (size_t)e[k].z*256 + f0);
-        float s0,s1,s2,s3; UNPK(s, s0,s1,s2,s3)
-        rf[k][0] += s0; rf[k][1] += s1; rf[k][2] += s2; rf[k][3] += s3;
-      }
-    }
-    #pragma unroll
-    for (int k = 0; k < 4; k++){
-      a0 += wv[k]*(bitsf(u[k].x << 16) + rf[k][0]);
-      a1 += wv[k]*(bitsf(u[k].x & 0xffff0000u) + rf[k][1]);
-      a2 += wv[k]*(bitsf(u[k].y << 16) + rf[k][2]);
-      a3 += wv[k]*(bitsf(u[k].y & 0xffff0000u) + rf[k][3]);
-    }
-  }
-  for (; t < en; t++){
-    float w = Wp[t];
-    int4 e = EIDX[t];
-    uint2 u = *(const uint2*)(P2 + (size_t)e.x*256 + f0);
-    uint2 rr = *(const uint2*)(PRm + (size_t)e.y*256 + f0);
-    float r0,r1,r2,r3; UNPK(rr, r0,r1,r2,r3)
-    if (e.z >= 0){
-      uint2 s = *(const uint2*)(PRm + (size_t)e.z*256 + f0);
-      float s0,s1,s2,s3; UNPK(s, s0,s1,s2,s3)
-      r0 += s0; r1 += s1; r2 += s2; r3 += s3;
-    }
-    a0 += w*(bitsf(u.x << 16) + r0);
-    a1 += w*(bitsf(u.x & 0xffff0000u) + r1);
-    a2 += w*(bitsf(u.y << 16) + r2);
-    a3 += w*(bitsf(u.y & 0xffff0000u) + r3);
-  }
-  float iv = IV1[i*4 + hf];
-  a0 *= iv; a1 *= iv; a2 *= iv; a3 *= iv;
-  float as = AS1[i*4 + hf];
-  uint2 up = *(const uint2*)(P1 + ob);
-  a0 += as*bitsf(up.x << 16);
-  a1 += as*bitsf(up.x & 0xffff0000u);
-  a2 += as*bitsf(up.y << 16);
-  a3 += as*bitsf(up.y & 0xffff0000u);
-  a0 = (a0 > 0.f) ? a0 : __expf(a0)-1.f;
-  a1 = (a1 > 0.f) ? a1 : __expf(a1)-1.f;
-  a2 = (a2 > 0.f) ? a2 : __expf(a2)-1.f;
-  a3 = (a3 > 0.f) ? a3 : __expf(a3)-1.f;
-  unsigned int lo = (unsigned int)bbits(a0) | ((unsigned int)bbits(a1) << 16);
-  unsigned int hi = (unsigned int)bbits(a2) | ((unsigned int)bbits(a3) << 16);
-  *(uint2*)(X1 + ob) = (uint2){lo, hi};
-}
-
-__global__ __launch_bounds__(256) void agg2(const int* __restrict__ off,
-    const int4* __restrict__ EIDX, const float* __restrict__ W2, const float* __restrict__ AS2,
-    const float* __restrict__ IV2,
-    const bf16* __restrict__ Q1, const bf16* __restrict__ Q2, const bf16* __restrict__ QRm,
-    const bf16* __restrict__ EP, float* __restrict__ X2){
-  __shared__ float red[4][256];
-  if (blockIdx.x < N_HEAVY){
-    int i = blockIdx.x;
-    int st = off[i], en = off[i+1];
-    if (en - st <= DEG_SPLIT) return;
-    int w = threadIdx.x >> 6, lane = threadIdx.x & 63;
-    int f0 = lane*4;
-    size_t ob = (size_t)i*256 + f0;
-    float a0=0,a1=0,a2=0,a3=0;
-    for (int t = st + w*4; t < en; t += 16){
-      int4 e[4]; float wv[4]; uint2 u[4]; uint2 rr[4];
-      #pragma unroll
-      for (int k = 0; k < 4; k++){
-        int tt = t + k;
-        bool vld = tt < en;
-        int tc = vld ? tt : st;
-        e[k] = EIDX[tc]; wv[k] = vld ? W2[tc] : 0.f;
-      }
-      #pragma unroll
-      for (int k = 0; k < 4; k++){
-        u[k] = *(const uint2*)(Q2 + (size_t)e[k].x*256 + f0);
-        rr[k] = *(const uint2*)(QRm + (size_t)e[k].y*256 + f0);
-      }
-      float rf[4][4];
-      #pragma unroll
-      for (int k = 0; k < 4; k++){ UNPK(rr[k], rf[k][0], rf[k][1], rf[k][2], rf[k][3]) }
-      #pragma unroll
-      for (int k = 0; k < 4; k++){
-        if (e[k].z >= 0){
-          uint2 s = *(const uint2*)(QRm + (size_t)e[k].z*256 + f0);
-          float s0,s1,s2,s3; UNPK(s, s0,s1,s2,s3)
-          rf[k][0] += s0; rf[k][1] += s1; rf[k][2] += s2; rf[k][3] += s3;
-        }
-      }
-      #pragma unroll
-      for (int k = 0; k < 4; k++){
-        a0 += wv[k]*(bitsf(u[k].x << 16) + rf[k][0]);
-        a1 += wv[k]*(bitsf(u[k].x & 0xffff0000u) + rf[k][1]);
-        a2 += wv[k]*(bitsf(u[k].y << 16) + rf[k][2]);
-        a3 += wv[k]*(bitsf(u[k].y & 0xffff0000u) + rf[k][3]);
-      }
-    }
-    *(float4*)&red[w][f0] = (float4){a0, a1, a2, a3};
-    __syncthreads();
-    if (w == 0){
-      float4 r1 = *(float4*)&red[1][f0];
-      float4 r2 = *(float4*)&red[2][f0];
-      float4 r3 = *(float4*)&red[3][f0];
-      a0 += r1.x + r2.x + r3.x;
-      a1 += r1.y + r2.y + r3.y;
-      a2 += r1.z + r2.z + r3.z;
-      a3 += r1.w + r2.w + r3.w;
-      float iv = IV2[i];
       a0 *= iv; a1 *= iv; a2 *= iv; a3 *= iv;
       float ep0=0.f, ep1=0.f, ep2=0.f, ep3=0.f;
       if (EP){
@@ -840,7 +846,6 @@
         ep0 = bitsf(ue.x << 16); ep1 = bitsf(ue.x & 0xffff0000u);
         ep2 = bitsf(ue.y << 16); ep3 = bitsf(ue.y & 0xffff0000u);
       }
-      float as = AS2[i];
       uint2 uq = *(const uint2*)(Q1 + ob);
       a0 += as*bitsf(uq.x << 16);
       a1 += as*bitsf(uq.x & 0xffff0000u);
@@ -871,56 +876,123 @@
     *(float4*)(X2 + ob) = (float4){ep0, ep1, ep2, ep3};
     return;
   }
+  float si = s1[i];
+  int deg = en - st;
   float a0=0,a1=0,a2=0,a3=0;
-  int t = st;
-  int n4 = st + ((en - st) & ~3);
-  for (; t < n4; t += 4){
-    int4 e[4]; float wv[4]; uint2 u[4]; uint2 rr[4];
-    #pragma unroll
-    for (int k = 0; k < 4; k++){ e[k] = EIDX[t+k]; wv[k] = W2[t+k]; }
-    #pragma unroll
-    for (int k = 0; k < 4; k++){
-      u[k] = *(const uint2*)(Q2 + (size_t)e[k].x*256 + f0);
-      rr[k] = *(const uint2*)(QRm + (size_t)e[k].y*256 + f0);
-    }
-    float rf[4][4];
-    #pragma unroll
-    for (int k = 0; k < 4; k++){ UNPK(rr[k], rf[k][0], rf[k][1], rf[k][2], rf[k][3]) }
-    #pragma unroll
-    for (int k = 0; k < 4; k++){
-      if (e[k].z >= 0){
-        uint2 s = *(const uint2*)(QRm + (size_t)e[k].z*256 + f0);
-        float s0,s1,s2,s3; UNPK(s, s0,s1,s2,s3)
-        rf[k][0] += s0; rf[k][1] += s1; rf[k][2] += s2; rf[k][3] += s3;
-      }
-    }
-    #pragma unroll
-    for (int k = 0; k < 4; k++){
-      a0 += wv[k]*(bitsf(u[k].x << 16) + rf[k][0]);
-      a1 += wv[k]*(bitsf(u[k].x & 0xffff0000u) + rf[k][1]);
-      a2 += wv[k]*(bitsf(u[k].y << 16) + rf[k][2]);
-      a3 += wv[k]*(bitsf(u[k].y & 0xffff0000u) + rf[k][3]);
-    }
-  }
-  for (; t < en; t++){
-    float w = W2[t];
-    int4 e = EIDX[t];
-    uint2 u = *(const uint2*)(Q2 + (size_t)e.x*256 + f0);
-    uint2 rr = *(const uint2*)(QRm + (size_t)e.y*256 + f0);
-    float r0,r1,r2,r3; UNPK(rr, r0,r1,r2,r3)
-    if (e.z >= 0){
-      uint2 s = *(const uint2*)(QRm + (size_t)e.z*256 + f0);
-      float s0,s1,s2,s3; UNPK(s, s0,s1,s2,s3)
-      r0 += s0; r1 += s1; r2 += s2; r3 += s3;
-    }
-    a0 += w*(bitsf(u.x << 16) + r0);
-    a1 += w*(bitsf(u.x & 0xffff0000u) + r1);
-    a2 += w*(bitsf(u.y << 16) + r2);
-    a3 += w*(bitsf(u.y & 0xffff0000u) + r3);
-  }
-  float iv = IV2[i];
+  float iv, as;
+  if (deg <= 64){
+    int t0 = st + lane;
+    float v0 = -1e30f;
+    if (t0 < en){
+      int4 e = EIDX[t0];
+      float v = si + s2[e.x] + sR[e.y];
+      if (e.z >= 0) v += sR[e.z];
+      v0 = (v >= 0.f) ? v : LRELU*v;
+    }
+    float mx = v0;
+    #pragma unroll
+    for (int o = 32; o >= 1; o >>= 1) mx = fmaxf(mx, __shfl_xor(mx, o, 64));
+    float ev0 = (t0 < en) ? __expf(v0 - mx) : 0.f;
+    float sm = ev0;
+    #pragma unroll
+    for (int o = 32; o >= 1; o >>= 1) sm += __shfl_xor(sm, o, 64);
+    iv = 1.f/(sm + 1e-16f);
+    as = sm*iv;
+    int t = st;
+    int n4 = st + (deg & ~3);
+    for (; t < n4; t += 4){
+      int j = t - st;
+      int4 e[4]; float wv[4]; uint2 u[4]; uint2 rr[4];
+      #pragma unroll
+      for (int k = 0; k < 4; k++){
+        e[k] = EIDX[t+k];
+        wv[k] = __shfl(ev0, j + k, 64);
+      }
+      #pragma unroll
+      for (int k = 0; k < 4; k++){
+        u[k] = *(const uint2*)(Q2 + (size_t)e[k].x*256 + f0);
+        rr[k] = *(const uint2*)(QRm + (size_t)e[k].y*256 + f0);
+      }
+      float rf[4][4];
+      #pragma unroll
+      for (int k = 0; k < 4; k++){ UNPK(rr[k], rf[k][0], rf[k][1], rf[k][2], rf[k][3]) }
+      #pragma unroll
+      for (int k = 0; k < 4; k++){
+        if (e[k].z >= 0){
+          uint2 s = *(const uint2*)(QRm + (size_t)e[k].z*256 + f0);
+          float s0,ss1,ss2,s3; UNPK(s, s0,ss1,ss2,s3)
+          rf[k][0] += s0; rf[k][1] += ss1; rf[k][2] += ss2; rf[k][3] += s3;
+        }
+      }
+      #pragma unroll
+      for (int k = 0; k < 4; k++){
+        a0 += wv[k]*(bitsf(u[k].x << 16) + rf[k][0]);
+        a1 += wv[k]*(bitsf(u[k].x & 0xffff0000u) + rf[k][1]);
+        a2 += wv[k]*(bitsf(u[k].y << 16) + rf[k][2]);
+        a3 += wv[k]*(bitsf(u[k].y & 0xffff0000u) + rf[k][3]);
+      }
+    }
+    for (; t < en; t++){
+      int j = t - st;
+      float w = __shfl(ev0, j, 64);
+      int4 e = EIDX[t];
+      uint2 u = *(const uint2*)(Q2 + (size_t)e.x*256 + f0);
+      uint2 rr = *(const uint2*)(QRm + (size_t)e.y*256 + f0);
+      float r0,r1,r2,r3; UNPK(rr, r0,r1,r2,r3)
+      if (e.z >= 0){
+        uint2 s = *(const uint2*)(QRm + (size_t)e.z*256 + f0);
+        float s0,ss1,ss2,s3; UNPK(s, s0,ss1,ss2,s3)
+        r0 += s0; r1 += ss1; r2 += ss2; r3 += s3;
+      }
+      a0 += w*(bitsf(u.x << 16) + r0);
+      a1 += w*(bitsf(u.x & 0xffff0000u) + r1);
+      a2 += w*(bitsf(u.y << 16) + r2);
+      a3 += w*(bitsf(u.y & 0xffff0000u) + r3);
+    }
+  } else {
+    float mx = -1e30f;
+    for (int t = st + lane; t < en; t += 64){
+      int4 e = EIDX[t];
+      float v = si + s2[e.x] + sR[e.y];
+      if (e.z >= 0) v += sR[e.z];
+      v = (v >= 0.f) ? v : LRELU*v;
+      mx = fmaxf(mx, v);
+    }
+    #pragma unroll
+    for (int o = 32; o >= 1; o >>= 1) mx = fmaxf(mx, __shfl_xor(mx, o, 64));
+    float sm = 0.f;
+    for (int t = st + lane; t < en; t += 64){
+      int4 e = EIDX[t];
+      float v = si + s2[e.x] + sR[e.y];
+      if (e.z >= 0) v += sR[e.z];
+      v = (v >= 0.f) ? v : LRELU*v;
+      sm += __expf(v - mx);
+    }
+    #pragma unroll
+    for (int o = 32; o >= 1; o >>= 1) sm += __shfl_xor(sm, o, 64);
+    iv = 1.f/(sm + 1e-16f);
+    as = sm*iv;
+    for (int t = st; t < en; t++){
+      int4 e = EIDX[t];
+      float v = si + s2[e.x] + sR[e.y];
+      if (e.z >= 0) v += sR[e.z];
+      v = (v >= 0.f) ? v : LRELU*v;
+      float w = __expf(v - mx);
+      uint2 u = *(const uint2*)(Q2 + (size_t)e.x*256 + f0);
+      uint2 rr = *(const uint2*)(QRm + (size_t)e.y*256 + f0);
+      float r0,r1,r2,r3; UNPK(rr, r0,r1,r2,r3)
+      if (e.z >= 0){
+        uint2 s = *(const uint2*)(QRm + (size_t)e.z*256 + f0);
+        float s0,ss1,ss2,s3; UNPK(s, s0,ss1,ss2,s3)
+        r0 += s0; r1 += ss1; r2 += ss2; r3 += s3;
+      }
+      a0 += w*(bitsf(u.x << 16) + r0);
+      a1 += w*(bitsf(u.x & 0xffff0000u) + r1);
+      a2 += w*(bitsf(u.y << 16) + r2);
+      a3 += w*(bitsf(u.y & 0xffff0000u) + r3);
+    }
+  }
   a0 *= iv; a1 *= iv; a2 *= iv; a3 *= iv;
-  float as = AS2[i];
   uint2 uq = *(const uint2*)(Q1 + ob);
   a0 += as*bitsf(uq.x << 16);
   a1 += as*bitsf(uq.x & 0xffff0000u);
@@ -1011,12 +1083,6 @@
   int*   B2O = (int*)alloc(16000);
   int*   C2  = (int*)alloc(2048);
   int4*  EIDX= (int4*)alloc(4000000);
-  float* L1  = (float*)alloc(4000000);
-  float* L2  = (float*)alloc(1000000);
-  float* AS1 = (float*)alloc(640000);
-  float* AS2 = (float*)alloc(160000);
-  float* IV1 = (float*)alloc(640000);
-  float* IV2 = (float*)alloc(160000);
   size_t base_end = o;
   bool useEP = (ws_size >= base_end + 20480256 + 512);
   bf16* EP = nullptr;
@@ -1041,15 +1107,13 @@
       rel, WC, gw, RF, SRm, PRb,
       ei, et, i2, OFF, CUR, B2O, EIDX, useEP ? 1 : 0);
 
-  sm1f<<<N_HEAVY + N_ENT/4, 256, 0, stream>>>(OFF, EIDX, S1, S2, SRm, L1, AS1, IV1);
-  agg1<<<N_HEAVY + N_ENT/4, 256, 0, stream>>>(OFF, EIDX, L1, AS1, IV1, P1, P2, PRb, X1b);
+  fag1<<<N_HEAVY + N_ENT/4, 256, 0, stream>>>(OFF, EIDX, S1, S2, SRm, P1, P2, PRb, X1b);
 
   mega2<<<32 + 2500, 256, 0, stream>>>(
       (const short*)X1b, (const short*)OWp0, (const short*)OWp1,
       P1, P2, oa, S1B, S2B, RF, ow + 131072, SRB, QRb);
 
-  sm2f<<<N_HEAVY + N_ENT/4, 256, 0, stream>>>(OFF, EIDX, S1B, S2B, SRB, L2, AS2, IV2);
-  agg2<<<N_HEAVY + N_ENT/4, 256, 0, stream>>>(OFF, EIDX, L2, AS2, IV2, P1, P2, QRb, EP, X2);
+  fag2<<<N_HEAVY + N_ENT/4, 256, 0, stream>>>(OFF, EIDX, S1B, S2B, SRB, P1, P2, QRb, EP, X2);
 
   if (!useEP)
     gemm64_acc<<<dim3((N_ENT+63)/64, 4), 256, 0, stream>>>(emb, we, X2, N_ENT, 128);
```
